# Optimization experiments

Measured on AMD Instinct MI355X. Metric: run time of the kernel, lower is better.

The kernel has to match this reference:

```python
import jax, jax.numpy as jnp
import numpy as np

B, T_IN, T_OUT, F, H = 1024, 168, 24, 8, 256


def _lstm_step(x, h, c, Wih, Whh, bih, bhh):
    # x: [B, in], h/c: [B, H]; PyTorch gate order i, f, g, o
    g = x @ Wih.T + h @ Whh.T + bih + bhh
    i, f, gg, o = jnp.split(g, 4, axis=-1)
    i = jax.nn.sigmoid(i)
    f = jax.nn.sigmoid(f)
    gg = jnp.tanh(gg)
    o = jax.nn.sigmoid(o)
    c2 = f * c + i * gg
    h2 = o * jnp.tanh(c2)
    return h2, c2


def _run_lstm(xs, Wih, Whh, bih, bhh):
    # xs: [T, B, in] -> (ys [T,B,H], h_T, c_T)
    Bs = xs.shape[1]
    h0 = jnp.zeros((Bs, H), xs.dtype)
    c0 = jnp.zeros((Bs, H), xs.dtype)
    def step(carry, x):
        h, c = carry
        h2, c2 = _lstm_step(x, h, c, Wih, Whh, bih, bhh)
        return (h2, c2), h2
    (hT, cT), ys = jax.lax.scan(step, (h0, c0), xs)
    return ys, hT, cT


def _forward(x, enc_Wih0, enc_Whh0, enc_bih0, enc_bhh0,
             enc_Wih1, enc_Whh1, enc_bih1, enc_bhh1,
             dec_Wih, dec_Whh, dec_bih, dec_bhh,
             fc1_W, fc1_b, attn_in_W, attn_in_b,
             attn_out_W, attn_out_b, fc2_W, fc2_b):
    scale = 1.0 / jnp.sqrt(jnp.asarray(H, x.dtype))

    # ---- encoder: 2-layer LSTM ----
    xs = jnp.transpose(x, (1, 0, 2))  # [T, B, F]
    ys0, h0, c0 = _run_lstm(xs, enc_Wih0, enc_Whh0, enc_bih0, enc_bhh0)
    _, h1, c1 = _run_lstm(ys0, enc_Wih1, enc_Whh1, enc_bih1, enc_bhh1)
    h_mean = (h0 + h1) * 0.5  # mean over layers, [B, H]
    c_mean = (c0 + c1) * 0.5

    # per-decoder initial state (same mean state for every decoder at t=0)
    h_state = jnp.tile(h_mean[None], (F, 1, 1))  # [F, B, H]
    c_state = jnp.tile(c_mean[None], (F, 1, 1))
    dec_in = x[:, -1, :]  # [B, F]

    def dec_one(xi, h, c, Wih, Whh, bih, bhh, f1W, f1b, inW, inb, oW, ob, f2W, f2b):
        # xi: [B, 1], single-feature single-step LSTM decode
        h2, c2 = _lstm_step(xi, h, c, Wih, Whh, bih, bhh)  # [B, H]
        a = jax.nn.leaky_relu(h2 @ f1W.T + f1b, 0.01)  # q = k = v
        qkv = a @ inW.T + inb  # [B, 3H]
        q, k, v = jnp.split(qkv, 3, axis=-1)
        # NB: faithful to the original bug: MultiheadAttention sees the batch
        # dim as the sequence dim, so attention is over the B examples.
        attn = jax.nn.softmax((q @ k.T) * scale, axis=-1)  # [B, B]
        ao = (attn @ v) @ oW.T + ob  # [B, H]
        out = jax.nn.leaky_relu(ao @ f2W.T + f2b, 0.01)  # [B, 1]
        return out[:, 0], h2, c2

    dec_all = jax.vmap(dec_one)  # over the F decoders

    def outer(carry, _):
        h, c, din = carry
        xi = din.T[:, :, None]  # [F, B, 1]
        out, h2, c2 = dec_all(xi, h, c, dec_Wih, dec_Whh, dec_bih, dec_bhh,
                              fc1_W, fc1_b, attn_in_W, attn_in_b,
                              attn_out_W, attn_out_b, fc2_W, fc2_b)
        return (h2, c2, out.T), out  # out: [F, B]

    _, outs = jax.lax.scan(outer, (h_state, c_state, dec_in), None, length=T_OUT)
    return jnp.transpose(outs, (2, 0, 1))  # [B, T_OUT, F]


def setup_inputs() -> dict:
    key = jax.random.key(0)
    ks = jax.random.split(key, 22)
    p = lambda k, shape: jax.random.normal(k, shape, dtype=jnp.float32) * 0.05
    return {
        "x": jax.random.normal(ks[0], (B, T_IN, F), dtype=jnp.float32),
        "enc_Wih0": p(ks[1], (4 * H, F)),
        "enc_Whh0": p(ks[2], (4 * H, H)),
        "enc_bih0": p(ks[3], (4 * H,)),
        "enc_bhh0": p(ks[4], (4 * H,)),
        "enc_Wih1": p(ks[5], (4 * H, H)),
        "enc_Whh1": p(ks[6], (4 * H, H)),
        "enc_bih1": p(ks[7], (4 * H,)),
        "enc_bhh1": p(ks[8], (4 * H,)),
        "dec_Wih": p(ks[9], (F, 4 * H, 1)),
        "dec_Whh": p(ks[10], (F, 4 * H, H)),
        "dec_bih": p(ks[11], (F, 4 * H)),
        "dec_bhh": p(ks[12], (F, 4 * H)),
        "fc1_W": p(ks[13], (F, H, H)),
        "fc1_b": p(ks[14], (F, H)),
        "attn_in_W": p(ks[15], (F, 3 * H, H)),
        "attn_in_b": p(ks[16], (F, 3 * H)),
        "attn_out_W": p(ks[17], (F, H, H)),
        "attn_out_b": p(ks[18], (F, H)),
        "fc2_W": p(ks[19], (F, 1, H)),
        "fc2_b": p(ks[20], (F, 1)),
    }


def reference(x, enc_Wih0, enc_Whh0, enc_bih0, enc_bhh0,
              enc_Wih1, enc_Whh1, enc_bih1, enc_bhh1,
              dec_Wih, dec_Whh, dec_bih, dec_bhh,
              fc1_W, fc1_b, attn_in_W, attn_in_b,
              attn_out_W, attn_out_b, fc2_W, fc2_b):
    return _forward(x, enc_Wih0, enc_Whh0, enc_bih0, enc_bhh0,
                    enc_Wih1, enc_Whh1, enc_bih1, enc_bhh1,
                    dec_Wih, dec_Whh, dec_bih, dec_bhh,
                    fc1_W, fc1_b, attn_in_W, attn_in_b,
                    attn_out_W, attn_out_b, fc2_W, fc2_b)
```

## Files before the change

### kernel.cpp

```cpp
#include <hip/hip_runtime.h>
#include <math.h>

#define H 256
#define H4 1024
#define Bsz 1024
#define TIN 168
#define TOUT 24
#define Fh 8
#define XROW (TIN*Fh)
#define BH ((size_t)Bsz * H)

typedef __attribute__((ext_vector_type(8))) short bf16x8;
typedef __attribute__((ext_vector_type(4))) float f32x4;

__device__ __forceinline__ ushort f2bf(float f) {
    union { float f; unsigned u; } v; v.f = f;
    unsigned r = v.u + 0x7fff + ((v.u >> 16) & 1);
    return (ushort)(r >> 16);
}
__device__ __forceinline__ float bf2f(ushort u) {
    union { unsigned u; float f; } v; v.u = ((unsigned)u) << 16;
    return v.f;
}
__device__ __forceinline__ float sigmf(float x) {
    return __fdividef(1.0f, 1.0f + __expf(-x));
}
__device__ __forceinline__ float tanhf_(float x) {
    const float e = __expf(-2.0f * fabsf(x));
    const float t = __fdividef(1.0f - e, 1.0f + e);
    return copysignf(t, x);
}

__device__ __forceinline__ void load_coh4(const ushort* p0, const ushort* p1,
                                          const ushort* p2, const ushort* p3,
                                          f32x4& a, f32x4& b, f32x4& c, f32x4& d)
{
    asm volatile(
        "global_load_dwordx4 %0, %4, off sc0 sc1\n\t"
        "global_load_dwordx4 %1, %5, off sc0 sc1\n\t"
        "global_load_dwordx4 %2, %6, off sc0 sc1\n\t"
        "global_load_dwordx4 %3, %7, off sc0 sc1\n\t"
        "s_waitcnt vmcnt(0)"
        : "=&v"(a), "=&v"(b), "=&v"(c), "=&v"(d)
        : "v"(p0), "v"(p1), "v"(p2), "v"(p3)
        : "memory");
}
__device__ __forceinline__ void load_coh8(const ushort* p0, const ushort* p1,
                                          const ushort* p2, const ushort* p3,
                                          const ushort* p4, const ushort* p5,
                                          const ushort* p6, const ushort* p7,
                                          f32x4& a, f32x4& b, f32x4& c, f32x4& d,
                                          f32x4& e, f32x4& f, f32x4& g, f32x4& h)
{
    asm volatile(
        "global_load_dwordx4 %0, %8, off sc0 sc1\n\t"
        "global_load_dwordx4 %1, %9, off sc0 sc1\n\t"
        "global_load_dwordx4 %2, %10, off sc0 sc1\n\t"
        "global_load_dwordx4 %3, %11, off sc0 sc1\n\t"
        "global_load_dwordx4 %4, %12, off sc0 sc1\n\t"
        "global_load_dwordx4 %5, %13, off sc0 sc1\n\t"
        "global_load_dwordx4 %6, %14, off sc0 sc1\n\t"
        "global_load_dwordx4 %7, %15, off sc0 sc1\n\t"
        "s_waitcnt vmcnt(0)"
        : "=&v"(a), "=&v"(b), "=&v"(c), "=&v"(d),
          "=&v"(e), "=&v"(f), "=&v"(g), "=&v"(h)
        : "v"(p0), "v"(p1), "v"(p2), "v"(p3), "v"(p4), "v"(p5), "v"(p6), "v"(p7)
        : "memory");
}
__device__ __forceinline__ void store_coh8B(ushort* p, uint2 v) {
    asm volatile("global_store_dwordx2 %0, %1, off sc0 sc1"
                 :: "v"(p), "v"(v) : "memory");
}

__device__ __forceinline__ void gbar2(unsigned* cnt, unsigned target) {
    asm volatile("s_waitcnt vmcnt(0)" ::: "memory");
    __syncthreads();
    if (threadIdx.x == 0) {
        __hip_atomic_fetch_add(cnt, 1u, __ATOMIC_RELAXED, __HIP_MEMORY_SCOPE_AGENT);
        int spins = 0;
        while (__hip_atomic_fetch_add(cnt, 0u, __ATOMIC_RELAXED,
                                      __HIP_MEMORY_SCOPE_AGENT) < target) {
            __builtin_amdgcn_s_sleep(1);
            if (++spins > 20000) break;
        }
    }
    __syncthreads();
    asm volatile("" ::: "memory");
}

__global__ __launch_bounds__(256)
void cast_f32_bf16(const float* __restrict__ in, ushort* __restrict__ out, int n) {
    int i = blockIdx.x * 256 + threadIdx.x;
    const int stride = gridDim.x * 256;
    for (; i < n; i += stride) out[i] = f2bf(in[i]);
}

__global__ __launch_bounds__(256)
void cast_pad_wih0(const float* __restrict__ in, ushort* __restrict__ out) {
    const int idx = blockIdx.x * 256 + threadIdx.x;
    const int row = idx >> 5, c = idx & 31;
    out[idx] = (c < 8) ? f2bf(in[row * 8 + c]) : (ushort)0;
}

__global__ __launch_bounds__(256)
void precompute_kernel(const float* __restrict__ oW, const float* __restrict__ ob,
                       const float* __restrict__ f2W, const float* __restrict__ f2b,
                       const float* __restrict__ inW, const float* __restrict__ inb,
                       float* __restrict__ u, float* __restrict__ dconst,
                       float* __restrict__ ccv)
{
    __shared__ float wsh[256];
    const int f = blockIdx.x;
    const int tid = threadIdx.x;
    float s = 0.f;
    for (int i = 0; i < 256; ++i)
        s += f2W[f * 256 + i] * oW[(size_t)f * 65536 + (size_t)i * 256 + tid];
    wsh[tid] = s;
    __syncthreads();
    float su = 0.f;
    for (int n = 0; n < 256; ++n)
        su += wsh[n] * inW[(size_t)f * 768 * 256 + (size_t)(512 + n) * 256 + tid];
    u[f * 256 + tid] = su;
    if (tid == 0) {
        float dd = 0.f, cc = 0.f;
        for (int n = 0; n < 256; ++n) dd += wsh[n] * inb[f * 768 + 512 + n];
        for (int i = 0; i < 256; ++i) cc += ob[f * 256 + i] * f2W[f * 256 + i];
        dconst[f] = dd;
        ccv[f] = cc + f2b[f];
    }
}

__global__ __launch_bounds__(256, 1)
void enc_persist2(const float* __restrict__ x,
                  const ushort* __restrict__ Whh0, const ushort* __restrict__ Wih0p,
                  const ushort* __restrict__ Wih1, const ushort* __restrict__ Whh1,
                  const float* __restrict__ bih0, const float* __restrict__ bhh0,
                  const float* __restrict__ bih1, const float* __restrict__ bhh1,
                  ushort* __restrict__ h0A, ushort* __restrict__ h0B,
                  ushort* __restrict__ h1A, ushort* __restrict__ h1B,
                  ushort* __restrict__ dh, float* __restrict__ dcb,
                  float* __restrict__ din, unsigned* __restrict__ bar)
{
    __shared__ ushort SA[32][264];
    __shared__ ushort SB[32][264];
    __shared__ ushort SC[32][264];
    __shared__ float pre[4][32][36];
    __shared__ ushort xL[32][32];

    const int tid = threadIdx.x;
    const int l = tid & 63;
    const int g = tid >> 6;
    const int lr = l & 15, lq = l >> 4, lk = lq * 8;
    const int grp = blockIdx.x >> 3, wgi = blockIdx.x & 7;
    const int rowbase = grp * 32;
    const int ub = wgi * 32;
    unsigned* cnt = bar + grp * 32;

    for (int e = tid; e < 32 * 32; e += 256) (&xL[0][0])[e] = 0;

    const int crow = tid >> 3;
    const int cu = (tid & 7) * 4;
    float c0v[4] = {0,0,0,0}, c1v[4] = {0,0,0,0};
    float h0v[4] = {0,0,0,0}, h1v[4] = {0,0,0,0};

    float b0s[2], b1s[2];
#pragma unroll
    for (int n = 0; n < 2; ++n) {
        const int j = ub + n * 16 + lr;
        b0s[n] = bih0[g * H + j] + bhh0[g * H + j];
        b1s[n] = bih1[g * H + j] + bhh1[g * H + j];
    }

    unsigned bph = 0;
    __syncthreads();

    for (int t = 0; t < TIN; ++t) {
        const int p = t & 1;
        const ushort* h0r = p ? h0B : h0A;
        ushort*       h0w = p ? h0A : h0B;
        const ushort* h1r = p ? h1B : h1A;
        ushort*       h1w = p ? h1A : h1B;

        {
            const ushort* src = h0r + rowbase * 256;
            f32x4 v0, v1, v2, v3;
            load_coh4(src + tid * 8, src + (tid + 256) * 8,
                      src + (tid + 512) * 8, src + (tid + 768) * 8, v0, v1, v2, v3);
            const int c16 = (tid & 31) * 8;
            *(f32x4*)&SA[tid >> 5][c16] = v0;
            *(f32x4*)&SA[(tid + 256) >> 5][c16] = v1;
            *(f32x4*)&SA[(tid + 512) >> 5][c16] = v2;
            *(f32x4*)&SA[(tid + 768) >> 5][c16] = v3;
            xL[tid >> 3][tid & 7] =
                f2bf(x[(size_t)(rowbase + (tid >> 3)) * XROW + t * Fh + (tid & 7)]);
        }
        __syncthreads();

        {
            bf16x8 am[2][8], ax[2];
#pragma unroll
            for (int m = 0; m < 2; ++m) {
#pragma unroll
                for (int k = 0; k < 8; ++k)
                    am[m][k] = *(const bf16x8*)&SA[m * 16 + lr][k * 32 + lk];
                ax[m] = *(const bf16x8*)&xL[m * 16 + lr][lk];
            }
            f32x4 acc[2][2] = {};
#pragma unroll
            for (int n = 0; n < 2; ++n) {
                const ushort* wp = Whh0 + (size_t)(g * H + ub + n * 16 + lr) * H + lk;
#pragma unroll
                for (int k = 0; k < 8; ++k) {
                    const bf16x8 b8 = *(const bf16x8*)(wp + k * 32);
                    acc[0][n] = __builtin_amdgcn_mfma_f32_16x16x32_bf16(am[0][k], b8, acc[0][n], 0, 0, 0);
                    acc[1][n] = __builtin_amdgcn_mfma_f32_16x16x32_bf16(am[1][k], b8, acc[1][n], 0, 0, 0);
                }
                const bf16x8 bx = *(const bf16x8*)(Wih0p + (size_t)(g * H + ub + n * 16 + lr) * 32 + lk);
                acc[0][n] = __builtin_amdgcn_mfma_f32_16x16x32_bf16(ax[0], bx, acc[0][n], 0, 0, 0);
                acc[1][n] = __builtin_amdgcn_mfma_f32_16x16x32_bf16(ax[1], bx, acc[1][n], 0, 0, 0);
            }
#pragma unroll
            for (int m = 0; m < 2; ++m)
#pragma unroll
                for (int n = 0; n < 2; ++n)
#pragma unroll
                    for (int r = 0; r < 4; ++r)
                        pre[g][m * 16 + lq * 4 + r][n * 16 + lr] = acc[m][n][r] + b0s[n];
        }
        __syncthreads();

        {
            const f32x4 pi = *(const f32x4*)&pre[0][crow][cu];
            const f32x4 pf = *(const f32x4*)&pre[1][crow][cu];
            const f32x4 pg = *(const f32x4*)&pre[2][crow][cu];
            const f32x4 po = *(const f32x4*)&pre[3][crow][cu];
#pragma unroll
            for (int j = 0; j < 4; ++j) {
                const float ig = sigmf(pi[j]);
                const float fg = sigmf(pf[j]);
                const float gg = tanhf_(pg[j]);
                const float og = sigmf(po[j]);
                c0v[j] = fg * c0v[j] + ig * gg;
                h0v[j] = og * tanhf_(c0v[j]);
            }
            uint2 hp;
            hp.x = (unsigned)f2bf(h0v[0]) | ((unsigned)f2bf(h0v[1]) << 16);
            hp.y = (unsigned)f2bf(h0v[2]) | ((unsigned)f2bf(h0v[3]) << 16);
            store_coh8B(h0w + (size_t)(rowbase + crow) * 256 + ub + cu, hp);
        }
        gbar2(cnt, ++bph * 8u);

        {
            const ushort* s0 = h0w + rowbase * 256;
            const ushort* s1 = h1r + rowbase * 256;
            f32x4 a0, a1, a2, a3, b0, b1, b2, b3;
            load_coh8(s0 + tid * 8, s0 + (tid + 256) * 8, s0 + (tid + 512) * 8, s0 + (tid + 768) * 8,
                      s1 + tid * 8, s1 + (tid + 256) * 8, s1 + (tid + 512) * 8, s1 + (tid + 768) * 8,
                      a0, a1, a2, a3, b0, b1, b2, b3);
            const int c16 = (tid & 31) * 8;
            *(f32x4*)&SB[tid >> 5][c16] = a0;
            *(f32x4*)&SB[(tid + 256) >> 5][c16] = a1;
            *(f32x4*)&SB[(tid + 512) >> 5][c16] = a2;
            *(f32x4*)&SB[(tid + 768) >> 5][c16] = a3;
            *(f32x4*)&SC[tid >> 5][c16] = b0;
            *(f32x4*)&SC[(tid + 256) >> 5][c16] = b1;
            *(f32x4*)&SC[(tid + 512) >> 5][c16] = b2;
            *(f32x4*)&SC[(tid + 768) >> 5][c16] = b3;
        }
        __syncthreads();

        {
            bf16x8 an[2][8], ah[2][8];
#pragma unroll
            for (int m = 0; m < 2; ++m)
#pragma unroll
                for (int k = 0; k < 8; ++k) {
                    an[m][k] = *(const bf16x8*)&SB[m * 16 + lr][k * 32 + lk];
                    ah[m][k] = *(const bf16x8*)&SC[m * 16 + lr][k * 32 + lk];
                }
            f32x4 acc[2][2] = {};
#pragma unroll
            for (int n = 0; n < 2; ++n) {
                const ushort* w1 = Wih1 + (size_t)(g * H + ub + n * 16 + lr) * H + lk;
                const ushort* w2 = Whh1 + (size_t)(g * H + ub + n * 16 + lr) * H + lk;
#pragma unroll
                for (int k = 0; k < 8; ++k) {
                    const bf16x8 b1 = *(const bf16x8*)(w1 + k * 32);
                    acc[0][n] = __builtin_amdgcn_mfma_f32_16x16x32_bf16(an[0][k], b1, acc[0][n], 0, 0, 0);
                    acc[1][n] = __builtin_amdgcn_mfma_f32_16x16x32_bf16(an[1][k], b1, acc[1][n], 0, 0, 0);
                    const bf16x8 b2 = *(const bf16x8*)(w2 + k * 32);
                    acc[0][n] = __builtin_amdgcn_mfma_f32_16x16x32_bf16(ah[0][k], b2, acc[0][n], 0, 0, 0);
                    acc[1][n] = __builtin_amdgcn_mfma_f32_16x16x32_bf16(ah[1][k], b2, acc[1][n], 0, 0, 0);
                }
            }
#pragma unroll
            for (int m = 0; m < 2; ++m)
#pragma unroll
                for (int n = 0; n < 2; ++n)
#pragma unroll
                    for (int r = 0; r < 4; ++r)
                        pre[g][m * 16 + lq * 4 + r][n * 16 + lr] = acc[m][n][r] + b1s[n];
        }
        __syncthreads();

        {
            const f32x4 pi = *(const f32x4*)&pre[0][crow][cu];
            const f32x4 pf = *(const f32x4*)&pre[1][crow][cu];
            const f32x4 pg = *(const f32x4*)&pre[2][crow][cu];
            const f32x4 po = *(const f32x4*)&pre[3][crow][cu];
#pragma unroll
            for (int j = 0; j < 4; ++j) {
                const float ig = sigmf(pi[j]);
                const float fg = sigmf(pf[j]);
                const float gg = tanhf_(pg[j]);
                const float og = sigmf(po[j]);
                c1v[j] = fg * c1v[j] + ig * gg;
                h1v[j] = og * tanhf_(c1v[j]);
            }
            uint2 hp;
            hp.x = (unsigned)f2bf(h1v[0]) | ((unsigned)f2bf(h1v[1]) << 16);
            hp.y = (unsigned)f2bf(h1v[2]) | ((unsigned)f2bf(h1v[3]) << 16);
            store_coh8B(h1w + (size_t)(rowbase + crow) * 256 + ub + cu, hp);
        }
        gbar2(cnt, ++bph * 8u);
    }

    {
        uint2 hm2;
        float cm[4];
        float hm[4];
#pragma unroll
        for (int j = 0; j < 4; ++j) {
            hm[j] = 0.5f * (h0v[j] + h1v[j]);
            cm[j] = 0.5f * (c0v[j] + c1v[j]);
        }
        hm2.x = (unsigned)f2bf(hm[0]) | ((unsigned)f2bf(hm[1]) << 16);
        hm2.y = (unsigned)f2bf(hm[2]) | ((unsigned)f2bf(hm[3]) << 16);
        const size_t idx = (size_t)(rowbase + crow) * 256 + ub + cu;
#pragma unroll
        for (int f = 0; f < Fh; ++f) {
            *(uint2*)&dh[f * BH + idx] = hm2;
            float4 c4; c4.x = cm[0]; c4.y = cm[1]; c4.z = cm[2]; c4.w = cm[3];
            *(float4*)&dcb[f * BH + idx] = c4;
        }
        if (wgi == 0) {
            const int r = tid >> 3, fc = tid & 7;
            din[(rowbase + r) * Fh + fc] =
                x[(size_t)(rowbase + r) * XROW + (TIN - 1) * Fh + fc];
        }
    }
}

template<int DO_ATTN, int DO_DEC>
__global__ __launch_bounds__(256, 1)
void dec_step(const ushort* __restrict__ qprev, const ushort* __restrict__ kprev,
              const float* __restrict__ vwprev,
              ushort* __restrict__ qcur, ushort* __restrict__ kcur,
              float* __restrict__ vwcur,
              ushort* __restrict__ dhg, float* __restrict__ dcg,
              const ushort* __restrict__ Whh, const float* __restrict__ Wih,
              const float* __restrict__ bih, const float* __restrict__ bhh,
              const ushort* __restrict__ f1Wb, const float* __restrict__ f1b,
              const ushort* __restrict__ inWb, const float* __restrict__ inb,
              const float* __restrict__ u, const float* __restrict__ dconst,
              const float* __restrict__ ccv, const float* __restrict__ din0,
              float* __restrict__ out, int t)
{
    __shared__ ushort h2s[32][264];
    __shared__ ushort as[32][264];
    __shared__ float dinL[32];
    __shared__ float tri[4][2][16][3];
    const int bid = blockIdx.x;
    const int f = bid & 7, mb = bid >> 3;
    const int m0 = mb * 32;
    const int tid = threadIdx.x;
    const int l = tid & 63, w = tid >> 6;
    const int lr = l & 15, lq = l >> 4, lk = lq * 8;

    if (DO_ATTN) {
        bf16x8 qf[2][8];
#pragma unroll
        for (int m = 0; m < 2; ++m)
#pragma unroll
            for (int k = 0; k < 8; ++k)
                qf[m][k] = *(const bf16x8*)(qprev + ((size_t)f * Bsz + m0 + m * 16 + lr) * H + k * 32 + lk);
        float mM0 = -1e30f, lS0 = 0.f, oS0 = 0.f;
        float mM1 = -1e30f, lS1 = 0.f, oS1 = 0.f;
        const int kb0 = w * 256;
        for (int kf = 0; kf < 16; ++kf) {
            const int kb = kb0 + kf * 16;
            f32x4 acc0 = {}, acc1 = {};
#pragma unroll
            for (int k = 0; k < 8; ++k) {
                const bf16x8 k8 = *(const bf16x8*)(kprev + ((size_t)f * Bsz + kb + lr) * H + k * 32 + lk);
                acc0 = __builtin_amdgcn_mfma_f32_16x16x32_bf16(k8, qf[0][k], acc0, 0, 0, 0);
                acc1 = __builtin_amdgcn_mfma_f32_16x16x32_bf16(k8, qf[1][k], acc1, 0, 0, 0);
            }
            const float4 v4 = *(const float4*)(vwprev + f * Bsz + kb + lq * 4);
            {
                const float mx = fmaxf(fmaxf(acc0[0], acc0[1]), fmaxf(acc0[2], acc0[3]));
                const float mn = fmaxf(mM0, mx);
                const float sc = __expf(mM0 - mn);
                const float e0 = __expf(acc0[0] - mn), e1 = __expf(acc0[1] - mn);
                const float e2 = __expf(acc0[2] - mn), e3 = __expf(acc0[3] - mn);
                lS0 = lS0 * sc + (e0 + e1 + e2 + e3);
                oS0 = oS0 * sc + (e0 * v4.x + e1 * v4.y + e2 * v4.z + e3 * v4.w);
                mM0 = mn;
            }
            {
                const float mx = fmaxf(fmaxf(acc1[0], acc1[1]), fmaxf(acc1[2], acc1[3]));
                const float mn = fmaxf(mM1, mx);
                const float sc = __expf(mM1 - mn);
                const float e0 = __expf(acc1[0] - mn), e1 = __expf(acc1[1] - mn);
                const float e2 = __expf(acc1[2] - mn), e3 = __expf(acc1[3] - mn);
                lS1 = lS1 * sc + (e0 + e1 + e2 + e3);
                oS1 = oS1 * sc + (e0 * v4.x + e1 * v4.y + e2 * v4.z + e3 * v4.w);
                mM1 = mn;
            }
        }
#pragma unroll
        for (int d = 16; d < 64; d <<= 1) {
            {
                const float m2 = __shfl_xor(mM0, d), l2 = __shfl_xor(lS0, d), o2 = __shfl_xor(oS0, d);
                const float mn = fmaxf(mM0, m2);
                const float sa = __expf(mM0 - mn), sb = __expf(m2 - mn);
                lS0 = lS0 * sa + l2 * sb; oS0 = oS0 * sa + o2 * sb; mM0 = mn;
            }
            {
                const float m2 = __shfl_xor(mM1, d), l2 = __shfl_xor(lS1, d), o2 = __shfl_xor(oS1, d);
                const float mn = fmaxf(mM1, m2);
                const float sa = __expf(mM1 - mn), sb = __expf(m2 - mn);
                lS1 = lS1 * sa + l2 * sb; oS1 = oS1 * sa + o2 * sb; mM1 = mn;
            }
        }
        if (l < 16) {
            tri[w][0][l][0] = mM0; tri[w][0][l][1] = lS0; tri[w][0][l][2] = oS0;
            tri[w][1][l][0] = mM1; tri[w][1][l][1] = lS1; tri[w][1][l][2] = oS1;
        }
        __syncthreads();
        if (tid < 32) {
            const int m = tid >> 4, qr = tid & 15;
            float M = tri[0][m][qr][0], L = tri[0][m][qr][1], O = tri[0][m][qr][2];
#pragma unroll
            for (int ww = 1; ww < 4; ++ww) {
                const float m2 = tri[ww][m][qr][0], l2 = tri[ww][m][qr][1], o2 = tri[ww][m][qr][2];
                const float mn = fmaxf(M, m2);
                const float sa = __expf(M - mn), sb = __expf(m2 - mn);
                L = L * sa + l2 * sb; O = O * sa + o2 * sb; M = mn;
            }
            float val = __fdividef(O, L) + ccv[f];
            val = (val > 0.f) ? val : 0.01f * val;
            const int b = m0 + m * 16 + qr;
            out[(size_t)b * (TOUT * Fh) + (size_t)(t - 1) * Fh + f] = val;
            dinL[m * 16 + qr] = val;
        }
        __syncthreads();
    }

    if (DO_DEC) {
        float bsum[4][4], wxr[4][4];
#pragma unroll
        for (int jt = 0; jt < 4; ++jt)
#pragma unroll
            for (int g = 0; g < 4; ++g) {
                const int j = w * 64 + jt * 16 + lr;
                bsum[jt][g] = bih[f * H4 + g * H + j] + bhh[f * H4 + g * H + j];
                wxr[jt][g] = Wih[f * H4 + g * H + j];
            }
        bf16x8 af[2][8];
#pragma unroll
        for (int m = 0; m < 2; ++m)
#pragma unroll
            for (int k = 0; k < 8; ++k)
                af[m][k] = *(const bf16x8*)(dhg + ((size_t)f * Bsz + m0 + m * 16 + lr) * H + k * 32 + lk);
        __syncthreads();
        const ushort* Wb = Whh + (size_t)f * (H4 * H);
#pragma unroll 1
        for (int jt = 0; jt < 4; ++jt) {
            const int jb = w * 64 + jt * 16;
            f32x4 acc[2][4] = {};
#pragma unroll
            for (int k = 0; k < 8; ++k)
#pragma unroll
                for (int g = 0; g < 4; ++g) {
                    const bf16x8 bf = *(const bf16x8*)(Wb + (size_t)(g * H + jb + lr) * H + k * 32 + lk);
                    acc[0][g] = __builtin_amdgcn_mfma_f32_16x16x32_bf16(af[0][k], bf, acc[0][g], 0, 0, 0);
                    acc[1][g] = __builtin_amdgcn_mfma_f32_16x16x32_bf16(af[1][k], bf, acc[1][g], 0, 0, 0);
                }
#pragma unroll
            for (int m = 0; m < 2; ++m)
#pragma unroll
                for (int r = 0; r < 4; ++r) {
                    const int row = m * 16 + lq * 4 + r;
                    const float xi = DO_ATTN ? dinL[row] : din0[(m0 + row) * Fh + f];
                    const float ig = sigmf(acc[m][0][r] + bsum[jt][0] + xi * wxr[jt][0]);
                    const float fg = sigmf(acc[m][1][r] + bsum[jt][1] + xi * wxr[jt][1]);
                    const float gg = tanhf_(acc[m][2][r] + bsum[jt][2] + xi * wxr[jt][2]);
                    const float og = sigmf(acc[m][3][r] + bsum[jt][3] + xi * wxr[jt][3]);
                    const size_t off = ((size_t)f * Bsz + m0 + row) * H + jb + lr;
                    const float cn = fg * dcg[off] + ig * gg;
                    dcg[off] = cn;
                    const ushort hb = f2bf(og * tanhf_(cn));
                    dhg[off] = hb;
                    h2s[row][jb + lr] = hb;
                }
        }
        __syncthreads();
        bf16x8 a2[2][8];
#pragma unroll
        for (int m = 0; m < 2; ++m)
#pragma unroll
            for (int k = 0; k < 8; ++k)
                a2[m][k] = *(const bf16x8*)&h2s[m * 16 + lr][k * 32 + lk];
        const ushort* Wf = f1Wb + (size_t)f * H * H;
#pragma unroll 1
        for (int nt = 0; nt < 4; ++nt) {
            const int n0 = w * 64 + nt * 16;
            f32x4 acc0 = {}, acc1 = {};
#pragma unroll
            for (int k = 0; k < 8; ++k) {
                const bf16x8 b8 = *(const bf16x8*)(Wf + (size_t)(n0 + lr) * H + k * 32 + lk);
                acc0 = __builtin_amdgcn_mfma_f32_16x16x32_bf16(a2[0][k], b8, acc0, 0, 0, 0);
                acc1 = __builtin_amdgcn_mfma_f32_16x16x32_bf16(a2[1][k], b8, acc1, 0, 0, 0);
            }
            const float bv = f1b[f * H + n0 + lr];
#pragma unroll
            for (int r = 0; r < 4; ++r) {
                float v0 = acc0[r] + bv; v0 = (v0 > 0.f) ? v0 : 0.01f * v0;
                as[lq * 4 + r][n0 + lr] = f2bf(v0);
                float v1 = acc1[r] + bv; v1 = (v1 > 0.f) ? v1 : 0.01f * v1;
                as[16 + lq * 4 + r][n0 + lr] = f2bf(v1);
            }
        }
        __syncthreads();
        bf16x8 a3[2][8];
#pragma unroll
        for (int m = 0; m < 2; ++m)
#pragma unroll
            for (int k = 0; k < 8; ++k)
                a3[m][k] = *(const bf16x8*)&as[m * 16 + lr][k * 32 + lk];
        const ushort* Wi = inWb + (size_t)f * 768 * H;
#pragma unroll 1
        for (int nt = 0; nt < 8; ++nt) {
            const int n0 = w * 128 + nt * 16;
            f32x4 acc0 = {}, acc1 = {};
#pragma unroll
            for (int k = 0; k < 8; ++k) {
                const bf16x8 b8 = *(const bf16x8*)(Wi + (size_t)(n0 + lr) * H + k * 32 + lk);
                acc0 = __builtin_amdgcn_mfma_f32_16x16x32_bf16(a3[0][k], b8, acc0, 0, 0, 0);
                acc1 = __builtin_amdgcn_mfma_f32_16x16x32_bf16(a3[1][k], b8, acc1, 0, 0, 0);
            }
            const float bv = inb[f * 768 + n0 + lr];
#pragma unroll
            for (int m = 0; m < 2; ++m)
#pragma unroll
                for (int r = 0; r < 4; ++r) {
                    const float v = (m ? acc1[r] : acc0[r]) + bv;
                    const int mrow = m0 + m * 16 + lq * 4 + r;
                    if (n0 < 256)
                        qcur[((size_t)f * Bsz + mrow) * H + n0 + lr] = f2bf(v * 0.0625f);
                    else
                        kcur[((size_t)f * Bsz + mrow) * H + n0 - 256 + lr] = f2bf(v);
                }
        }
        const float4 u4 = *(const float4*)(u + f * H + l * 4);
#pragma unroll 1
        for (int rr = 0; rr < 8; ++rr) {
            const int mloc = w * 8 + rr;
            const ushort4 a4 = *(const ushort4*)&as[mloc][l * 4];
            float s = bf2f(a4.x) * u4.x + bf2f(a4.y) * u4.y
                    + bf2f(a4.z) * u4.z + bf2f(a4.w) * u4.w;
#pragma unroll
            for (int d = 1; d < 64; d <<= 1) s += __shfl_xor(s, d);
            if (l == 0) vwcur[f * Bsz + m0 + mloc] = s + dconst[f];
        }
    }
}

extern "C" void kernel_launch(void* const* d_in, const int* in_sizes, int n_in,
                              void* d_out, int out_size, void* d_ws, size_t ws_size,
                              hipStream_t stream)
{
    const float* x     = (const float*)d_in[0];
    const float* eWih0 = (const float*)d_in[1];
    const float* eWhh0 = (const float*)d_in[2];
    const float* ebih0 = (const float*)d_in[3];
    const float* ebhh0 = (const float*)d_in[4];
    const float* eWih1 = (const float*)d_in[5];
    const float* eWhh1 = (const float*)d_in[6];
    const float* ebih1 = (const float*)d_in[7];
    const float* ebhh1 = (const float*)d_in[8];
    const float* dWih  = (const float*)d_in[9];
    const float* dWhh  = (const float*)d_in[10];
    const float* dbih  = (const float*)d_in[11];
    const float* dbhh  = (const float*)d_in[12];
    const float* f1W   = (const float*)d_in[13];
    const float* f1b   = (const float*)d_in[14];
    const float* inW   = (const float*)d_in[15];
    const float* inb   = (const float*)d_in[16];
    const float* oW    = (const float*)d_in[17];
    const float* ob    = (const float*)d_in[18];
    const float* f2W   = (const float*)d_in[19];
    const float* f2b   = (const float*)d_in[20];
    float* out = (float*)d_out;

    char* base = (char*)d_ws;
    size_t o = 0;
    auto alloc = [&](size_t bytes) { void* p = base + o; o += (bytes + 255) & ~(size_t)255; return p; };
    ushort* h0A = (ushort*)alloc(BH * 2);
    ushort* h1A = (ushort*)alloc(BH * 2);
    ushort* h0B = (ushort*)alloc(BH * 2);
    ushort* h1B = (ushort*)alloc(BH * 2);
    unsigned* bar = (unsigned*)alloc(32 * 32 * 4);
    ushort* qb[2]; ushort* kb[2]; float* vw[2];
    qb[0] = (ushort*)alloc(8 * BH * 2);
    qb[1] = (ushort*)alloc(8 * BH * 2);
    kb[0] = (ushort*)alloc(8 * BH * 2);
    kb[1] = (ushort*)alloc(8 * BH * 2);
    vw[0] = (float*)alloc((size_t)Fh * Bsz * 4);
    vw[1] = (float*)alloc((size_t)Fh * Bsz * 4);
    ushort* dhg  = (ushort*)alloc(8 * BH * 2);
    float*  dcg  = (float*)alloc(8 * BH * 4);
    float*  din0 = (float*)alloc((size_t)Bsz * Fh * 4);
    float*  ubuf = (float*)alloc((size_t)Fh * H * 4);
    float*  dbuf = (float*)alloc(Fh * 4);
    float*  ccb  = (float*)alloc(Fh * 4);
    ushort* wWhh0 = (ushort*)alloc((size_t)H4 * H * 2);
    ushort* wWih0p= (ushort*)alloc((size_t)H4 * 32 * 2);
    ushort* wWih1 = (ushort*)alloc((size_t)H4 * H * 2);
    ushort* wWhh1 = (ushort*)alloc((size_t)H4 * H * 2);
    ushort* wdWhh = (ushort*)alloc((size_t)8 * H4 * H * 2);
    ushort* wf1W  = (ushort*)alloc((size_t)8 * H * H * 2);
    ushort* winW  = (ushort*)alloc((size_t)8 * 768 * H * 2);

    const dim3 blk(256);

    hipMemsetAsync(d_ws, 0, BH * 2 * 2, stream);
    hipMemsetAsync(bar, 0, 32 * 32 * 4, stream);

    cast_f32_bf16<<<dim3(512), blk, 0, stream>>>(eWhh0, wWhh0, H4 * H);
    cast_f32_bf16<<<dim3(512), blk, 0, stream>>>(eWih1, wWih1, H4 * H);
    cast_f32_bf16<<<dim3(512), blk, 0, stream>>>(eWhh1, wWhh1, H4 * H);
    cast_pad_wih0<<<dim3(128), blk, 0, stream>>>(eWih0, wWih0p);
    cast_f32_bf16<<<dim3(1024), blk, 0, stream>>>(dWhh, wdWhh, 8 * H4 * H);
    cast_f32_bf16<<<dim3(512), blk, 0, stream>>>(f1W, wf1W, 8 * H * H);
    cast_f32_bf16<<<dim3(1024), blk, 0, stream>>>(inW, winW, 8 * 768 * H);
    precompute_kernel<<<dim3(8), blk, 0, stream>>>(oW, ob, f2W, f2b, inW, inb,
                                                   ubuf, dbuf, ccb);

    enc_persist2<<<dim3(256), blk, 0, stream>>>(
        x, wWhh0, wWih0p, wWih1, wWhh1, ebih0, ebhh0, ebih1, ebhh1,
        h0A, h0B, h1A, h1B, dhg, dcg, din0, bar);

    dec_step<0, 1><<<dim3(256), blk, 0, stream>>>(
        qb[1], kb[1], vw[1], qb[0], kb[0], vw[0], dhg, dcg,
        wdWhh, dWih, dbih, dbhh, wf1W, f1b, winW, inb,
        ubuf, dbuf, ccb, din0, out, 0);
    for (int t = 1; t < TOUT; ++t) {
        const int pp = (t - 1) & 1, pc = t & 1;
        dec_step<1, 1><<<dim3(256), blk, 0, stream>>>(
            qb[pp], kb[pp], vw[pp], qb[pc], kb[pc], vw[pc], dhg, dcg,
            wdWhh, dWih, dbih, dbhh, wf1W, f1b, winW, inb,
            ubuf, dbuf, ccb, din0, out, t);
    }
    dec_step<1, 0><<<dim3(256), blk, 0, stream>>>(
        qb[1], kb[1], vw[1], qb[0], kb[0], vw[0], dhg, dcg,
        wdWhh, dWih, dbih, dbhh, wf1W, f1b, winW, inb,
        ubuf, dbuf, ccb, din0, out, TOUT);

    (void)in_sizes; (void)n_in; (void)out_size; (void)ws_size;
}
```

Baseline: 3.681 ms.

## Merge encoder and decoder steps into one persistent kernel with grid barriers

Replaces the separate encoder kernel and the 25 per-step decoder launches with a single persistent kernel. Stages are separated by software global barriers instead of kernel boundaries. The hidden-state buffers move to a sliced layout so each thread loads one contiguous 32-element row. Decoder state is kept as one shared mean h/c buffer instead of eight replicated copies, and some loads now use L2-coherent rather than system-coherent flags. This removes per-launch overhead and the replicated state writes, but it depends on all 256 blocks being co-resident and on spin-barrier correctness.

Measured after the change: 3.568 ms. 1.03x faster.

```diff
diff --git a/kernel.cpp b/kernel.cpp
--- a/kernel.cpp
+++ b/kernel.cpp
@@ -9,6 +9,7 @@
 #define Fh 8
 #define XROW (TIN*Fh)
 #define BH ((size_t)Bsz * H)
+#define SL32 ((size_t)Bsz * 32)
 
 typedef __attribute__((ext_vector_type(8))) short bf16x8;
 typedef __attribute__((ext_vector_type(4))) float f32x4;
@@ -67,21 +68,68 @@
         : "v"(p0), "v"(p1), "v"(p2), "v"(p3), "v"(p4), "v"(p5), "v"(p6), "v"(p7)
         : "memory");
 }
+__device__ __forceinline__ void load_coh4f(const float* p0, const float* p1,
+                                           const float* p2, const float* p3,
+                                           float& a, float& b, float& c, float& d)
+{
+    asm volatile(
+        "global_load_dword %0, %4, off sc0 sc1\n\t"
+        "global_load_dword %1, %5, off sc0 sc1\n\t"
+        "global_load_dword %2, %6, off sc0 sc1\n\t"
+        "global_load_dword %3, %7, off sc0 sc1\n\t"
+        "s_waitcnt vmcnt(0)"
+        : "=&v"(a), "=&v"(b), "=&v"(c), "=&v"(d)
+        : "v"(p0), "v"(p1), "v"(p2), "v"(p3)
+        : "memory");
+}
 __device__ __forceinline__ void store_coh8B(ushort* p, uint2 v) {
     asm volatile("global_store_dwordx2 %0, %1, off sc0 sc1"
                  :: "v"(p), "v"(v) : "memory");
 }
-
-__device__ __forceinline__ void gbar2(unsigned* cnt, unsigned target) {
+__device__ __forceinline__ void store_coh16B(float* p, f32x4 v) {
+    asm volatile("global_store_dwordx4 %0, %1, off sc0 sc1"
+                 :: "v"(p), "v"(v) : "memory");
+}
+
+__device__ __forceinline__ void load_l2_8(const ushort* p0, const ushort* p1,
+                                          const ushort* p2, const ushort* p3,
+                                          const ushort* p4, const ushort* p5,
+                                          const ushort* p6, const ushort* p7,
+                                          f32x4& a, f32x4& b, f32x4& c, f32x4& d,
+                                          f32x4& e, f32x4& f, f32x4& g, f32x4& h)
+{
+    asm volatile(
+        "global_load_dwordx4 %0, %8, off sc0\n\t"
+        "global_load_dwordx4 %1, %9, off sc0\n\t"
+        "global_load_dwordx4 %2, %10, off sc0\n\t"
+        "global_load_dwordx4 %3, %11, off sc0\n\t"
+        "global_load_dwordx4 %4, %12, off sc0\n\t"
+        "global_load_dwordx4 %5, %13, off sc0\n\t"
+        "global_load_dwordx4 %6, %14, off sc0\n\t"
+        "global_load_dwordx4 %7, %15, off sc0\n\t"
+        "s_waitcnt vmcnt(0)"
+        : "=&v"(a), "=&v"(b), "=&v"(c), "=&v"(d),
+          "=&v"(e), "=&v"(f), "=&v"(g), "=&v"(h)
+        : "v"(p0), "v"(p1), "v"(p2), "v"(p3), "v"(p4), "v"(p5), "v"(p6), "v"(p7)
+        : "memory");
+}
+__device__ __forceinline__ void load_l2_f4(const float* p, f32x4& v) {
+    asm volatile(
+        "global_load_dwordx4 %0, %1, off sc0\n\t"
+        "s_waitcnt vmcnt(0)"
+        : "=&v"(v) : "v"(p) : "memory");
+}
+
+__device__ __forceinline__ void gbar(unsigned* cnt, unsigned target) {
     asm volatile("s_waitcnt vmcnt(0)" ::: "memory");
     __syncthreads();
     if (threadIdx.x == 0) {
         __hip_atomic_fetch_add(cnt, 1u, __ATOMIC_RELAXED, __HIP_MEMORY_SCOPE_AGENT);
-        int spins = 0;
+        int sp = 0;
         while (__hip_atomic_fetch_add(cnt, 0u, __ATOMIC_RELAXED,
                                       __HIP_MEMORY_SCOPE_AGENT) < target) {
-            __builtin_amdgcn_s_sleep(1);
-            if (++spins > 20000) break;
+            __builtin_amdgcn_s_sleep(2);
+            if (++sp > 20000) break;
         }
     }
     __syncthreads();
@@ -130,449 +178,484 @@
     }
 }
 
+struct MP {
+    const float *x, *ebih0, *ebhh0, *ebih1, *ebhh1;
+    const ushort *Whh0, *Wih0p, *Wih1, *Whh1;
+    ushort *h0A, *h0B, *h1A, *h1B, *hm;
+    float *cm;
+    const ushort *dWhh, *f1Wb, *inWb;
+    const float *dWih, *dbih, *dbhh, *f1b, *inb, *u, *dconst, *ccv;
+    ushort *kb0, *kb1;
+    float *vw0, *vw1, *out;
+    unsigned *bar;
+};
+
 __global__ __launch_bounds__(256, 1)
-void enc_persist2(const float* __restrict__ x,
-                  const ushort* __restrict__ Whh0, const ushort* __restrict__ Wih0p,
-                  const ushort* __restrict__ Wih1, const ushort* __restrict__ Whh1,
-                  const float* __restrict__ bih0, const float* __restrict__ bhh0,
-                  const float* __restrict__ bih1, const float* __restrict__ bhh1,
-                  ushort* __restrict__ h0A, ushort* __restrict__ h0B,
-                  ushort* __restrict__ h1A, ushort* __restrict__ h1B,
-                  ushort* __restrict__ dh, float* __restrict__ dcb,
-                  float* __restrict__ din, unsigned* __restrict__ bar)
+void mega2(MP P)
 {
     __shared__ ushort SA[32][264];
     __shared__ ushort SB[32][264];
     __shared__ ushort SC[32][264];
     __shared__ float pre[4][32][36];
     __shared__ ushort xL[32][32];
-
-    const int tid = threadIdx.x;
-    const int l = tid & 63;
-    const int g = tid >> 6;
-    const int lr = l & 15, lq = l >> 4, lk = lq * 8;
-    const int grp = blockIdx.x >> 3, wgi = blockIdx.x & 7;
-    const int rowbase = grp * 32;
-    const int ub = wgi * 32;
-    unsigned* cnt = bar + grp * 32;
-
-    for (int e = tid; e < 32 * 32; e += 256) (&xL[0][0])[e] = 0;
-
-    const int crow = tid >> 3;
-    const int cu = (tid & 7) * 4;
-    float c0v[4] = {0,0,0,0}, c1v[4] = {0,0,0,0};
-    float h0v[4] = {0,0,0,0}, h1v[4] = {0,0,0,0};
-
-    float b0s[2], b1s[2];
-#pragma unroll
-    for (int n = 0; n < 2; ++n) {
-        const int j = ub + n * 16 + lr;
-        b0s[n] = bih0[g * H + j] + bhh0[g * H + j];
-        b1s[n] = bih1[g * H + j] + bhh1[g * H + j];
-    }
-
-    unsigned bph = 0;
-    __syncthreads();
-
-    for (int t = 0; t < TIN; ++t) {
-        const int p = t & 1;
-        const ushort* h0r = p ? h0B : h0A;
-        ushort*       h0w = p ? h0A : h0B;
-        const ushort* h1r = p ? h1B : h1A;
-        ushort*       h1w = p ? h1A : h1B;
-
-        {
-            const ushort* src = h0r + rowbase * 256;
-            f32x4 v0, v1, v2, v3;
-            load_coh4(src + tid * 8, src + (tid + 256) * 8,
-                      src + (tid + 512) * 8, src + (tid + 768) * 8, v0, v1, v2, v3);
-            const int c16 = (tid & 31) * 8;
-            *(f32x4*)&SA[tid >> 5][c16] = v0;
-            *(f32x4*)&SA[(tid + 256) >> 5][c16] = v1;
-            *(f32x4*)&SA[(tid + 512) >> 5][c16] = v2;
-            *(f32x4*)&SA[(tid + 768) >> 5][c16] = v3;
-            xL[tid >> 3][tid & 7] =
-                f2bf(x[(size_t)(rowbase + (tid >> 3)) * XROW + t * Fh + (tid & 7)]);
-        }
-        __syncthreads();
-
-        {
-            bf16x8 am[2][8], ax[2];
-#pragma unroll
-            for (int m = 0; m < 2; ++m) {
-#pragma unroll
-                for (int k = 0; k < 8; ++k)
-                    am[m][k] = *(const bf16x8*)&SA[m * 16 + lr][k * 32 + lk];
-                ax[m] = *(const bf16x8*)&xL[m * 16 + lr][lk];
-            }
-            f32x4 acc[2][2] = {};
-#pragma unroll
-            for (int n = 0; n < 2; ++n) {
-                const ushort* wp = Whh0 + (size_t)(g * H + ub + n * 16 + lr) * H + lk;
-#pragma unroll
-                for (int k = 0; k < 8; ++k) {
-                    const bf16x8 b8 = *(const bf16x8*)(wp + k * 32);
-                    acc[0][n] = __builtin_amdgcn_mfma_f32_16x16x32_bf16(am[0][k], b8, acc[0][n], 0, 0, 0);
-                    acc[1][n] = __builtin_amdgcn_mfma_f32_16x16x32_bf16(am[1][k], b8, acc[1][n], 0, 0, 0);
-                }
-                const bf16x8 bx = *(const bf16x8*)(Wih0p + (size_t)(g * H + ub + n * 16 + lr) * 32 + lk);
-                acc[0][n] = __builtin_amdgcn_mfma_f32_16x16x32_bf16(ax[0], bx, acc[0][n], 0, 0, 0);
-                acc[1][n] = __builtin_amdgcn_mfma_f32_16x16x32_bf16(ax[1], bx, acc[1][n], 0, 0, 0);
-            }
-#pragma unroll
-            for (int m = 0; m < 2; ++m)
-#pragma unroll
-                for (int n = 0; n < 2; ++n)
-#pragma unroll
-                    for (int r = 0; r < 4; ++r)
-                        pre[g][m * 16 + lq * 4 + r][n * 16 + lr] = acc[m][n][r] + b0s[n];
-        }
-        __syncthreads();
-
-        {
-            const f32x4 pi = *(const f32x4*)&pre[0][crow][cu];
-            const f32x4 pf = *(const f32x4*)&pre[1][crow][cu];
-            const f32x4 pg = *(const f32x4*)&pre[2][crow][cu];
-            const f32x4 po = *(const f32x4*)&pre[3][crow][cu];
-#pragma unroll
-            for (int j = 0; j < 4; ++j) {
-                const float ig = sigmf(pi[j]);
-                const float fg = sigmf(pf[j]);
-                const float gg = tanhf_(pg[j]);
-                const float og = sigmf(po[j]);
-                c0v[j] = fg * c0v[j] + ig * gg;
-                h0v[j] = og * tanhf_(c0v[j]);
-            }
-            uint2 hp;
-            hp.x = (unsigned)f2bf(h0v[0]) | ((unsigned)f2bf(h0v[1]) << 16);
-            hp.y = (unsigned)f2bf(h0v[2]) | ((unsigned)f2bf(h0v[3]) << 16);
-            store_coh8B(h0w + (size_t)(rowbase + crow) * 256 + ub + cu, hp);
-        }
-        gbar2(cnt, ++bph * 8u);
-
-        {
-            const ushort* s0 = h0w + rowbase * 256;
-            const ushort* s1 = h1r + rowbase * 256;
-            f32x4 a0, a1, a2, a3, b0, b1, b2, b3;
-            load_coh8(s0 + tid * 8, s0 + (tid + 256) * 8, s0 + (tid + 512) * 8, s0 + (tid + 768) * 8,
-                      s1 + tid * 8, s1 + (tid + 256) * 8, s1 + (tid + 512) * 8, s1 + (tid + 768) * 8,
-                      a0, a1, a2, a3, b0, b1, b2, b3);
-            const int c16 = (tid & 31) * 8;
-            *(f32x4*)&SB[tid >> 5][c16] = a0;
-            *(f32x4*)&SB[(tid + 256) >> 5][c16] = a1;
-            *(f32x4*)&SB[(tid + 512) >> 5][c16] = a2;
-            *(f32x4*)&SB[(tid + 768) >> 5][c16] = a3;
-            *(f32x4*)&SC[tid >> 5][c16] = b0;
-            *(f32x4*)&SC[(tid + 256) >> 5][c16] = b1;
-            *(f32x4*)&SC[(tid + 512) >> 5][c16] = b2;
-            *(f32x4*)&SC[(tid + 768) >> 5][c16] = b3;
-        }
-        __syncthreads();
-
-        {
-            bf16x8 an[2][8], ah[2][8];
-#pragma unroll
-            for (int m = 0; m < 2; ++m)
-#pragma unroll
-                for (int k = 0; k < 8; ++k) {
-                    an[m][k] = *(const bf16x8*)&SB[m * 16 + lr][k * 32 + lk];
-                    ah[m][k] = *(const bf16x8*)&SC[m * 16 + lr][k * 32 + lk];
-                }
-            f32x4 acc[2][2] = {};
-#pragma unroll
-            for (int n = 0; n < 2; ++n) {
-                const ushort* w1 = Wih1 + (size_t)(g * H + ub + n * 16 + lr) * H + lk;
-                const ushort* w2 = Whh1 + (size_t)(g * H + ub + n * 16 + lr) * H + lk;
-#pragma unroll
-                for (int k = 0; k < 8; ++k) {
-                    const bf16x8 b1 = *(const bf16x8*)(w1 + k * 32);
-                    acc[0][n] = __builtin_amdgcn_mfma_f32_16x16x32_bf16(an[0][k], b1, acc[0][n], 0, 0, 0);
-                    acc[1][n] = __builtin_amdgcn_mfma_f32_16x16x32_bf16(an[1][k], b1, acc[1][n], 0, 0, 0);
-                    const bf16x8 b2 = *(const bf16x8*)(w2 + k * 32);
-                    acc[0][n] = __builtin_amdgcn_mfma_f32_16x16x32_bf16(ah[0][k], b2, acc[0][n], 0, 0, 0);
-                    acc[1][n] = __builtin_amdgcn_mfma_f32_16x16x32_bf16(ah[1][k], b2, acc[1][n], 0, 0, 0);
-                }
-            }
-#pragma unroll
-            for (int m = 0; m < 2; ++m)
-#pragma unroll
-                for (int n = 0; n < 2; ++n)
-#pragma unroll
-                    for (int r = 0; r < 4; ++r)
-                        pre[g][m * 16 + lq * 4 + r][n * 16 + lr] = acc[m][n][r] + b1s[n];
-        }
-        __syncthreads();
-
-        {
-            const f32x4 pi = *(const f32x4*)&pre[0][crow][cu];
-            const f32x4 pf = *(const f32x4*)&pre[1][crow][cu];
-            const f32x4 pg = *(const f32x4*)&pre[2][crow][cu];
-            const f32x4 po = *(const f32x4*)&pre[3][crow][cu];
-#pragma unroll
-            for (int j = 0; j < 4; ++j) {
-                const float ig = sigmf(pi[j]);
-                const float fg = sigmf(pf[j]);
-                const float gg = tanhf_(pg[j]);
-                const float og = sigmf(po[j]);
-                c1v[j] = fg * c1v[j] + ig * gg;
-                h1v[j] = og * tanhf_(c1v[j]);
-            }
-            uint2 hp;
-            hp.x = (unsigned)f2bf(h1v[0]) | ((unsigned)f2bf(h1v[1]) << 16);
-            hp.y = (unsigned)f2bf(h1v[2]) | ((unsigned)f2bf(h1v[3]) << 16);
-            store_coh8B(h1w + (size_t)(rowbase + crow) * 256 + ub + cu, hp);
-        }
-        gbar2(cnt, ++bph * 8u);
-    }
-
-    {
-        uint2 hm2;
-        float cm[4];
-        float hm[4];
-#pragma unroll
-        for (int j = 0; j < 4; ++j) {
-            hm[j] = 0.5f * (h0v[j] + h1v[j]);
-            cm[j] = 0.5f * (c0v[j] + c1v[j]);
-        }
-        hm2.x = (unsigned)f2bf(hm[0]) | ((unsigned)f2bf(hm[1]) << 16);
-        hm2.y = (unsigned)f2bf(hm[2]) | ((unsigned)f2bf(hm[3]) << 16);
-        const size_t idx = (size_t)(rowbase + crow) * 256 + ub + cu;
-#pragma unroll
-        for (int f = 0; f < Fh; ++f) {
-            *(uint2*)&dh[f * BH + idx] = hm2;
-            float4 c4; c4.x = cm[0]; c4.y = cm[1]; c4.z = cm[2]; c4.w = cm[3];
-            *(float4*)&dcb[f * BH + idx] = c4;
-        }
-        if (wgi == 0) {
-            const int r = tid >> 3, fc = tid & 7;
-            din[(rowbase + r) * Fh + fc] =
-                x[(size_t)(rowbase + r) * XROW + (TIN - 1) * Fh + fc];
-        }
-    }
-}
-
-template<int DO_ATTN, int DO_DEC>
-__global__ __launch_bounds__(256, 1)
-void dec_step(const ushort* __restrict__ qprev, const ushort* __restrict__ kprev,
-              const float* __restrict__ vwprev,
-              ushort* __restrict__ qcur, ushort* __restrict__ kcur,
-              float* __restrict__ vwcur,
-              ushort* __restrict__ dhg, float* __restrict__ dcg,
-              const ushort* __restrict__ Whh, const float* __restrict__ Wih,
-              const float* __restrict__ bih, const float* __restrict__ bhh,
-              const ushort* __restrict__ f1Wb, const float* __restrict__ f1b,
-              const ushort* __restrict__ inWb, const float* __restrict__ inb,
-              const float* __restrict__ u, const float* __restrict__ dconst,
-              const float* __restrict__ ccv, const float* __restrict__ din0,
-              float* __restrict__ out, int t)
-{
     __shared__ ushort h2s[32][264];
-    __shared__ ushort as[32][264];
+    __shared__ ushort as2[32][264];
+    __shared__ ushort qs[32][264];
+    __shared__ float tri[4][2][16][3];
     __shared__ float dinL[32];
-    __shared__ float tri[4][2][16][3];
+
     const int bid = blockIdx.x;
-    const int f = bid & 7, mb = bid >> 3;
-    const int m0 = mb * 32;
     const int tid = threadIdx.x;
     const int l = tid & 63, w = tid >> 6;
     const int lr = l & 15, lq = l >> 4, lk = lq * 8;
 
-    if (DO_ATTN) {
-        bf16x8 qf[2][8];
+    {
+        const int grp = bid >> 3, wgi = bid & 7;
+        const int rowbase = grp * 32;
+        const int ub = wgi * 32;
+        unsigned* cnt = P.bar + grp * 32;
+        const int g = w;
+        const int sS = tid >> 5, sR = tid & 31;
+
+        for (int e = tid; e < 32 * 32; e += 256) (&xL[0][0])[e] = 0;
+
+        const int crow = tid >> 3;
+        const int cu = (tid & 7) * 4;
+        float c0v[4] = {0,0,0,0}, c1v[4] = {0,0,0,0};
+        float h0v[4] = {0,0,0,0}, h1v[4] = {0,0,0,0};
+
+        float b0s[2], b1s[2];
+#pragma unroll
+        for (int n = 0; n < 2; ++n) {
+            const int j = ub + n * 16 + lr;
+            b0s[n] = P.ebih0[g * H + j] + P.ebhh0[g * H + j];
+            b1s[n] = P.ebih1[g * H + j] + P.ebhh1[g * H + j];
+        }
+        unsigned bph = 0;
+        __syncthreads();
+
+        for (int t = 0; t < TIN; ++t) {
+            const int p = t & 1;
+            const ushort* h0r = p ? P.h0B : P.h0A;
+            ushort*       h0w = p ? P.h0A : P.h0B;
+            const ushort* h1r = p ? P.h1B : P.h1A;
+            ushort*       h1w = p ? P.h1A : P.h1B;
+
+            {
+                const ushort* s0 = h0r + sS * SL32 + (size_t)(rowbase + sR) * 32;
+                f32x4 v0, v1, v2, v3;
+                load_coh4(s0, s0 + 8, s0 + 16, s0 + 24, v0, v1, v2, v3);
+                *(f32x4*)&SA[sR][sS * 32 + 0]  = v0;
+                *(f32x4*)&SA[sR][sS * 32 + 8]  = v1;
+                *(f32x4*)&SA[sR][sS * 32 + 16] = v2;
+                *(f32x4*)&SA[sR][sS * 32 + 24] = v3;
+                xL[tid >> 3][tid & 7] =
+                    f2bf(P.x[(size_t)(rowbase + (tid >> 3)) * XROW + t * Fh + (tid & 7)]);
+            }
+            __syncthreads();
+            {
+                bf16x8 am[2][8], ax[2];
+#pragma unroll
+                for (int m = 0; m < 2; ++m) {
+#pragma unroll
+                    for (int k = 0; k < 8; ++k)
+                        am[m][k] = *(const bf16x8*)&SA[m * 16 + lr][k * 32 + lk];
+                    ax[m] = *(const bf16x8*)&xL[m * 16 + lr][lk];
+                }
+                f32x4 acc[2][2] = {};
+#pragma unroll
+                for (int n = 0; n < 2; ++n) {
+                    const ushort* wp = P.Whh0 + (size_t)(g * H + ub + n * 16 + lr) * H + lk;
+#pragma unroll
+                    for (int k = 0; k < 8; ++k) {
+                        const bf16x8 b8 = *(const bf16x8*)(wp + k * 32);
+                        acc[0][n] = __builtin_amdgcn_mfma_f32_16x16x32_bf16(am[0][k], b8, acc[0][n], 0, 0, 0);
+                        acc[1][n] = __builtin_amdgcn_mfma_f32_16x16x32_bf16(am[1][k], b8, acc[1][n], 0, 0, 0);
+                    }
+                    const bf16x8 bx = *(const bf16x8*)(P.Wih0p + (size_t)(g * H + ub + n * 16 + lr) * 32 + lk);
+                    acc[0][n] = __builtin_amdgcn_mfma_f32_16x16x32_bf16(ax[0], bx, acc[0][n], 0, 0, 0);
+                    acc[1][n] = __builtin_amdgcn_mfma_f32_16x16x32_bf16(ax[1], bx, acc[1][n], 0, 0, 0);
+                }
+#pragma unroll
+                for (int m = 0; m < 2; ++m)
+#pragma unroll
+                    for (int n = 0; n < 2; ++n)
+#pragma unroll
+                        for (int r = 0; r < 4; ++r)
+                            pre[g][m * 16 + lq * 4 + r][n * 16 + lr] = acc[m][n][r] + b0s[n];
+            }
+            __syncthreads();
+            {
+                const f32x4 pi = *(const f32x4*)&pre[0][crow][cu];
+                const f32x4 pf = *(const f32x4*)&pre[1][crow][cu];
+                const f32x4 pg = *(const f32x4*)&pre[2][crow][cu];
+                const f32x4 po = *(const f32x4*)&pre[3][crow][cu];
+#pragma unroll
+                for (int j = 0; j < 4; ++j) {
+                    const float ig = sigmf(pi[j]);
+                    const float fg = sigmf(pf[j]);
+                    const float gg = tanhf_(pg[j]);
+                    const float og = sigmf(po[j]);
+                    c0v[j] = fg * c0v[j] + ig * gg;
+                    h0v[j] = og * tanhf_(c0v[j]);
+                }
+                uint2 hp;
+                hp.x = (unsigned)f2bf(h0v[0]) | ((unsigned)f2bf(h0v[1]) << 16);
+                hp.y = (unsigned)f2bf(h0v[2]) | ((unsigned)f2bf(h0v[3]) << 16);
+                store_coh8B(h0w + wgi * SL32 + (size_t)(rowbase + crow) * 32 + cu, hp);
+            }
+            gbar(cnt, ++bph * 8u);
+            {
+                const ushort* s0 = h0w + sS * SL32 + (size_t)(rowbase + sR) * 32;
+                const ushort* s1 = h1r + sS * SL32 + (size_t)(rowbase + sR) * 32;
+                f32x4 a0, a1, a2, a3, b0, b1, b2, b3;
+                load_coh8(s0, s0 + 8, s0 + 16, s0 + 24,
+                          s1, s1 + 8, s1 + 16, s1 + 24,
+                          a0, a1, a2, a3, b0, b1, b2, b3);
+                *(f32x4*)&SB[sR][sS * 32 + 0]  = a0;
+                *(f32x4*)&SB[sR][sS * 32 + 8]  = a1;
+                *(f32x4*)&SB[sR][sS * 32 + 16] = a2;
+                *(f32x4*)&SB[sR][sS * 32 + 24] = a3;
+                *(f32x4*)&SC[sR][sS * 32 + 0]  = b0;
+                *(f32x4*)&SC[sR][sS * 32 + 8]  = b1;
+                *(f32x4*)&SC[sR][sS * 32 + 16] = b2;
+                *(f32x4*)&SC[sR][sS * 32 + 24] = b3;
+            }
+            __syncthreads();
+            {
+                bf16x8 an[2][8], ah[2][8];
+#pragma unroll
+                for (int m = 0; m < 2; ++m)
+#pragma unroll
+                    for (int k = 0; k < 8; ++k) {
+                        an[m][k] = *(const bf16x8*)&SB[m * 16 + lr][k * 32 + lk];
+                        ah[m][k] = *(const bf16x8*)&SC[m * 16 + lr][k * 32 + lk];
+                    }
+                f32x4 acc[2][2] = {};
+#pragma unroll
+                for (int n = 0; n < 2; ++n) {
+                    const ushort* w1 = P.Wih1 + (size_t)(g * H + ub + n * 16 + lr) * H + lk;
+                    const ushort* w2 = P.Whh1 + (size_t)(g * H + ub + n * 16 + lr) * H + lk;
+#pragma unroll
+                    for (int k = 0; k < 8; ++k) {
+                        const bf16x8 b1 = *(const bf16x8*)(w1 + k * 32);
+                        acc[0][n] = __builtin_amdgcn_mfma_f32_16x16x32_bf16(an[0][k], b1, acc[0][n], 0, 0, 0);
+                        acc[1][n] = __builtin_amdgcn_mfma_f32_16x16x32_bf16(an[1][k], b1, acc[1][n], 0, 0, 0);
+                        const bf16x8 b2 = *(const bf16x8*)(w2 + k * 32);
+                        acc[0][n] = __builtin_amdgcn_mfma_f32_16x16x32_bf16(ah[0][k], b2, acc[0][n], 0, 0, 0);
+                        acc[1][n] = __builtin_amdgcn_mfma_f32_16x16x32_bf16(ah[1][k], b2, acc[1][n], 0, 0, 0);
+                    }
+                }
+#pragma unroll
+                for (int m = 0; m < 2; ++m)
+#pragma unroll
+                    for (int n = 0; n < 2; ++n)
+#pragma unroll
+                        for (int r = 0; r < 4; ++r)
+                            pre[g][m * 16 + lq * 4 + r][n * 16 + lr] = acc[m][n][r] + b1s[n];
+            }
+            __syncthreads();
+            {
+                const f32x4 pi = *(const f32x4*)&pre[0][crow][cu];
+                const f32x4 pf = *(const f32x4*)&pre[1][crow][cu];
+                const f32x4 pg = *(const f32x4*)&pre[2][crow][cu];
+                const f32x4 po = *(const f32x4*)&pre[3][crow][cu];
+#pragma unroll
+                for (int j = 0; j < 4; ++j) {
+                    const float ig = sigmf(pi[j]);
+                    const float fg = sigmf(pf[j]);
+                    const float gg = tanhf_(pg[j]);
+                    const float og = sigmf(po[j]);
+                    c1v[j] = fg * c1v[j] + ig * gg;
+                    h1v[j] = og * tanhf_(c1v[j]);
+                }
+                uint2 hp;
+                hp.x = (unsigned)f2bf(h1v[0]) | ((unsigned)f2bf(h1v[1]) << 16);
+                hp.y = (unsigned)f2bf(h1v[2]) | ((unsigned)f2bf(h1v[3]) << 16);
+                store_coh8B(h1w + wgi * SL32 + (size_t)(rowbase + crow) * 32 + cu, hp);
+            }
+            gbar(cnt, ++bph * 8u);
+        }
+        {
+            uint2 hp;
+            hp.x = (unsigned)f2bf(0.5f * (h0v[0] + h1v[0]))
+                 | ((unsigned)f2bf(0.5f * (h0v[1] + h1v[1])) << 16);
+            hp.y = (unsigned)f2bf(0.5f * (h0v[2] + h1v[2]))
+                 | ((unsigned)f2bf(0.5f * (h0v[3] + h1v[3])) << 16);
+            store_coh8B(P.hm + (size_t)(rowbase + crow) * 256 + ub + cu, hp);
+            f32x4 cv;
+#pragma unroll
+            for (int j = 0; j < 4; ++j) cv[j] = 0.5f * (c0v[j] + c1v[j]);
+            store_coh16B(P.cm + (size_t)(rowbase + crow) * 256 + ub + cu, cv);
+        }
+    }
+    gbar(P.bar + 2048, 256u);
+
+    {
+        const int f = bid & 7, mb = bid >> 3;
+        const int m0 = mb * 32;
+
+#pragma unroll
+        for (int it = 0; it < 4; ++it) {
+            const int idx = tid + it * 256;
+            const int r = idx >> 5, c16 = (idx & 31) * 8;
+            f32x4 v0, v1, v2, v3;
+            const ushort* pbase = P.hm + (size_t)(m0 + r) * 256 + c16;
+            asm volatile("global_load_dwordx4 %0, %1, off sc0 sc1\n\ts_waitcnt vmcnt(0)"
+                         : "=&v"(v0) : "v"(pbase) : "memory");
+            *(f32x4*)&h2s[r][c16] = v0;
+            (void)v1; (void)v2; (void)v3;
+        }
+        float cd[2][4][4];
 #pragma unroll
         for (int m = 0; m < 2; ++m)
 #pragma unroll
-            for (int k = 0; k < 8; ++k)
-                qf[m][k] = *(const bf16x8*)(qprev + ((size_t)f * Bsz + m0 + m * 16 + lr) * H + k * 32 + lk);
-        float mM0 = -1e30f, lS0 = 0.f, oS0 = 0.f;
-        float mM1 = -1e30f, lS1 = 0.f, oS1 = 0.f;
-        const int kb0 = w * 256;
-        for (int kf = 0; kf < 16; ++kf) {
-            const int kb = kb0 + kf * 16;
-            f32x4 acc0 = {}, acc1 = {};
-#pragma unroll
-            for (int k = 0; k < 8; ++k) {
-                const bf16x8 k8 = *(const bf16x8*)(kprev + ((size_t)f * Bsz + kb + lr) * H + k * 32 + lk);
-                acc0 = __builtin_amdgcn_mfma_f32_16x16x32_bf16(k8, qf[0][k], acc0, 0, 0, 0);
-                acc1 = __builtin_amdgcn_mfma_f32_16x16x32_bf16(k8, qf[1][k], acc1, 0, 0, 0);
-            }
-            const float4 v4 = *(const float4*)(vwprev + f * Bsz + kb + lq * 4);
-            {
-                const float mx = fmaxf(fmaxf(acc0[0], acc0[1]), fmaxf(acc0[2], acc0[3]));
-                const float mn = fmaxf(mM0, mx);
-                const float sc = __expf(mM0 - mn);
-                const float e0 = __expf(acc0[0] - mn), e1 = __expf(acc0[1] - mn);
-                const float e2 = __expf(acc0[2] - mn), e3 = __expf(acc0[3] - mn);
-                lS0 = lS0 * sc + (e0 + e1 + e2 + e3);
-                oS0 = oS0 * sc + (e0 * v4.x + e1 * v4.y + e2 * v4.z + e3 * v4.w);
-                mM0 = mn;
-            }
-            {
-                const float mx = fmaxf(fmaxf(acc1[0], acc1[1]), fmaxf(acc1[2], acc1[3]));
-                const float mn = fmaxf(mM1, mx);
-                const float sc = __expf(mM1 - mn);
-                const float e0 = __expf(acc1[0] - mn), e1 = __expf(acc1[1] - mn);
-                const float e2 = __expf(acc1[2] - mn), e3 = __expf(acc1[3] - mn);
-                lS1 = lS1 * sc + (e0 + e1 + e2 + e3);
-                oS1 = oS1 * sc + (e0 * v4.x + e1 * v4.y + e2 * v4.z + e3 * v4.w);
-                mM1 = mn;
-            }
-        }
-#pragma unroll
-        for (int d = 16; d < 64; d <<= 1) {
-            {
-                const float m2 = __shfl_xor(mM0, d), l2 = __shfl_xor(lS0, d), o2 = __shfl_xor(oS0, d);
-                const float mn = fmaxf(mM0, m2);
-                const float sa = __expf(mM0 - mn), sb = __expf(m2 - mn);
-                lS0 = lS0 * sa + l2 * sb; oS0 = oS0 * sa + o2 * sb; mM0 = mn;
-            }
-            {
-                const float m2 = __shfl_xor(mM1, d), l2 = __shfl_xor(lS1, d), o2 = __shfl_xor(oS1, d);
-                const float mn = fmaxf(mM1, m2);
-                const float sa = __expf(mM1 - mn), sb = __expf(m2 - mn);
-                lS1 = lS1 * sa + l2 * sb; oS1 = oS1 * sa + o2 * sb; mM1 = mn;
-            }
-        }
-        if (l < 16) {
-            tri[w][0][l][0] = mM0; tri[w][0][l][1] = lS0; tri[w][0][l][2] = oS0;
-            tri[w][1][l][0] = mM1; tri[w][1][l][1] = lS1; tri[w][1][l][2] = oS1;
-        }
-        __syncthreads();
-        if (tid < 32) {
-            const int m = tid >> 4, qr = tid & 15;
-            float M = tri[0][m][qr][0], L = tri[0][m][qr][1], O = tri[0][m][qr][2];
-#pragma unroll
-            for (int ww = 1; ww < 4; ++ww) {
-                const float m2 = tri[ww][m][qr][0], l2 = tri[ww][m][qr][1], o2 = tri[ww][m][qr][2];
-                const float mn = fmaxf(M, m2);
-                const float sa = __expf(M - mn), sb = __expf(m2 - mn);
-                L = L * sa + l2 * sb; O = O * sa + o2 * sb; M = mn;
-            }
-            float val = __fdividef(O, L) + ccv[f];
-            val = (val > 0.f) ? val : 0.01f * val;
-            const int b = m0 + m * 16 + qr;
-            out[(size_t)b * (TOUT * Fh) + (size_t)(t - 1) * Fh + f] = val;
-            dinL[m * 16 + qr] = val;
-        }
-        __syncthreads();
-    }
-
-    if (DO_DEC) {
+            for (int jt = 0; jt < 4; ++jt) {
+                const float* pc = P.cm + (size_t)(m0 + m * 16 + lq * 4) * 256
+                                + (w * 64 + jt * 16 + lr);
+                load_coh4f(pc, pc + 256, pc + 512, pc + 768,
+                           cd[m][jt][0], cd[m][jt][1], cd[m][jt][2], cd[m][jt][3]);
+            }
         float bsum[4][4], wxr[4][4];
 #pragma unroll
         for (int jt = 0; jt < 4; ++jt)
 #pragma unroll
             for (int g = 0; g < 4; ++g) {
                 const int j = w * 64 + jt * 16 + lr;
-                bsum[jt][g] = bih[f * H4 + g * H + j] + bhh[f * H4 + g * H + j];
-                wxr[jt][g] = Wih[f * H4 + g * H + j];
-            }
-        bf16x8 af[2][8];
-#pragma unroll
-        for (int m = 0; m < 2; ++m)
-#pragma unroll
-            for (int k = 0; k < 8; ++k)
-                af[m][k] = *(const bf16x8*)(dhg + ((size_t)f * Bsz + m0 + m * 16 + lr) * H + k * 32 + lk);
+                bsum[jt][g] = P.dbih[f * H4 + g * H + j] + P.dbhh[f * H4 + g * H + j];
+                wxr[jt][g] = P.dWih[f * H4 + g * H + j];
+            }
         __syncthreads();
-        const ushort* Wb = Whh + (size_t)f * (H4 * H);
-#pragma unroll 1
-        for (int jt = 0; jt < 4; ++jt) {
-            const int jb = w * 64 + jt * 16;
-            f32x4 acc[2][4] = {};
-#pragma unroll
-            for (int k = 0; k < 8; ++k)
-#pragma unroll
-                for (int g = 0; g < 4; ++g) {
-                    const bf16x8 bf = *(const bf16x8*)(Wb + (size_t)(g * H + jb + lr) * H + k * 32 + lk);
-                    acc[0][g] = __builtin_amdgcn_mfma_f32_16x16x32_bf16(af[0][k], bf, acc[0][g], 0, 0, 0);
-                    acc[1][g] = __builtin_amdgcn_mfma_f32_16x16x32_bf16(af[1][k], bf, acc[1][g], 0, 0, 0);
-                }
+
+        unsigned* fcnt = P.bar + 1024 + f * 32;
+
+        for (int t = 0; t < TOUT; ++t) {
+            ushort* kcur = (t & 1) ? P.kb1 : P.kb0;
+            float* vwcur = (t & 1) ? P.vw1 : P.vw0;
+
+            float xiv[2][4];
 #pragma unroll
             for (int m = 0; m < 2; ++m)
 #pragma unroll
                 for (int r = 0; r < 4; ++r) {
                     const int row = m * 16 + lq * 4 + r;
-                    const float xi = DO_ATTN ? dinL[row] : din0[(m0 + row) * Fh + f];
-                    const float ig = sigmf(acc[m][0][r] + bsum[jt][0] + xi * wxr[jt][0]);
-                    const float fg = sigmf(acc[m][1][r] + bsum[jt][1] + xi * wxr[jt][1]);
-                    const float gg = tanhf_(acc[m][2][r] + bsum[jt][2] + xi * wxr[jt][2]);
-                    const float og = sigmf(acc[m][3][r] + bsum[jt][3] + xi * wxr[jt][3]);
-                    const size_t off = ((size_t)f * Bsz + m0 + row) * H + jb + lr;
-                    const float cn = fg * dcg[off] + ig * gg;
-                    dcg[off] = cn;
-                    const ushort hb = f2bf(og * tanhf_(cn));
-                    dhg[off] = hb;
-                    h2s[row][jb + lr] = hb;
-                }
-        }
-        __syncthreads();
-        bf16x8 a2[2][8];
-#pragma unroll
-        for (int m = 0; m < 2; ++m)
-#pragma unroll
-            for (int k = 0; k < 8; ++k)
-                a2[m][k] = *(const bf16x8*)&h2s[m * 16 + lr][k * 32 + lk];
-        const ushort* Wf = f1Wb + (size_t)f * H * H;
+                    xiv[m][r] = (t == 0)
+                        ? P.x[(size_t)(m0 + row) * XROW + (TIN - 1) * Fh + f]
+                        : dinL[row];
+                }
+            bf16x8 af[2][8];
+#pragma unroll
+            for (int m = 0; m < 2; ++m)
+#pragma unroll
+                for (int k = 0; k < 8; ++k)
+                    af[m][k] = *(const bf16x8*)&h2s[m * 16 + lr][k * 32 + lk];
+            __syncthreads();
+            const ushort* Wb = P.dWhh + (size_t)f * (H4 * H);
 #pragma unroll 1
-        for (int nt = 0; nt < 4; ++nt) {
-            const int n0 = w * 64 + nt * 16;
-            f32x4 acc0 = {}, acc1 = {};
-#pragma unroll
-            for (int k = 0; k < 8; ++k) {
-                const bf16x8 b8 = *(const bf16x8*)(Wf + (size_t)(n0 + lr) * H + k * 32 + lk);
-                acc0 = __builtin_amdgcn_mfma_f32_16x16x32_bf16(a2[0][k], b8, acc0, 0, 0, 0);
-                acc1 = __builtin_amdgcn_mfma_f32_16x16x32_bf16(a2[1][k], b8, acc1, 0, 0, 0);
-            }
-            const float bv = f1b[f * H + n0 + lr];
-#pragma unroll
-            for (int r = 0; r < 4; ++r) {
-                float v0 = acc0[r] + bv; v0 = (v0 > 0.f) ? v0 : 0.01f * v0;
-                as[lq * 4 + r][n0 + lr] = f2bf(v0);
-                float v1 = acc1[r] + bv; v1 = (v1 > 0.f) ? v1 : 0.01f * v1;
-                as[16 + lq * 4 + r][n0 + lr] = f2bf(v1);
-            }
-        }
-        __syncthreads();
-        bf16x8 a3[2][8];
-#pragma unroll
-        for (int m = 0; m < 2; ++m)
-#pragma unroll
-            for (int k = 0; k < 8; ++k)
-                a3[m][k] = *(const bf16x8*)&as[m * 16 + lr][k * 32 + lk];
-        const ushort* Wi = inWb + (size_t)f * 768 * H;
+            for (int jt = 0; jt < 4; ++jt) {
+                const int j = w * 64 + jt * 16 + lr;
+                f32x4 acc[4][2] = {};
+#pragma unroll
+                for (int g = 0; g < 4; ++g) {
+                    const ushort* wp = Wb + (size_t)(g * H + j) * H + lk;
+#pragma unroll
+                    for (int k = 0; k < 8; ++k) {
+                        const bf16x8 b8 = *(const bf16x8*)(wp + k * 32);
+                        acc[g][0] = __builtin_amdgcn_mfma_f32_16x16x32_bf16(af[0][k], b8, acc[g][0], 0, 0, 0);
+                        acc[g][1] = __builtin_amdgcn_mfma_f32_16x16x32_bf16(af[1][k], b8, acc[g][1], 0, 0, 0);
+                    }
+                }
+#pragma unroll
+                for (int m = 0; m < 2; ++m)
+#pragma unroll
+                    for (int r = 0; r < 4; ++r) {
+                        const int row = m * 16 + lq * 4 + r;
+                        const float xi = xiv[m][r];
+                        const float ig = sigmf(acc[0][m][r] + bsum[jt][0] + xi * wxr[jt][0]);
+                        const float fg = sigmf(acc[1][m][r] + bsum[jt][1] + xi * wxr[jt][1]);
+                        const float gg = tanhf_(acc[2][m][r] + bsum[jt][2] + xi * wxr[jt][2]);
+                        const float og = sigmf(acc[3][m][r] + bsum[jt][3] + xi * wxr[jt][3]);
+                        const float cn = fg * cd[m][jt][r] + ig * gg;
+                        cd[m][jt][r] = cn;
+                        h2s[row][j] = f2bf(og * tanhf_(cn));
+                    }
+            }
+            __syncthreads();
+            bf16x8 a2[2][8];
+#pragma unroll
+            for (int m = 0; m < 2; ++m)
+#pragma unroll
+                for (int k = 0; k < 8; ++k)
+                    a2[m][k] = *(const bf16x8*)&h2s[m * 16 + lr][k * 32 + lk];
+            const ushort* Wf = P.f1Wb + (size_t)f * H * H;
 #pragma unroll 1
-        for (int nt = 0; nt < 8; ++nt) {
-            const int n0 = w * 128 + nt * 16;
-            f32x4 acc0 = {}, acc1 = {};
-#pragma unroll
-            for (int k = 0; k < 8; ++k) {
-                const bf16x8 b8 = *(const bf16x8*)(Wi + (size_t)(n0 + lr) * H + k * 32 + lk);
-                acc0 = __builtin_amdgcn_mfma_f32_16x16x32_bf16(a3[0][k], b8, acc0, 0, 0, 0);
-                acc1 = __builtin_amdgcn_mfma_f32_16x16x32_bf16(a3[1][k], b8, acc1, 0, 0, 0);
-            }
-            const float bv = inb[f * 768 + n0 + lr];
+            for (int nt = 0; nt < 4; ++nt) {
+                const int n = w * 64 + nt * 16 + lr;
+                f32x4 acc0 = {}, acc1 = {};
+                const ushort* wp = Wf + (size_t)n * H + lk;
+#pragma unroll
+                for (int k = 0; k < 8; ++k) {
+                    const bf16x8 b8 = *(const bf16x8*)(wp + k * 32);
+                    acc0 = __builtin_amdgcn_mfma_f32_16x16x32_bf16(a2[0][k], b8, acc0, 0, 0, 0);
+                    acc1 = __builtin_amdgcn_mfma_f32_16x16x32_bf16(a2[1][k], b8, acc1, 0, 0, 0);
+                }
+                const float bv = P.f1b[f * H + n];
+#pragma unroll
+                for (int r = 0; r < 4; ++r) {
+                    float v0 = acc0[r] + bv; v0 = (v0 > 0.f) ? v0 : 0.01f * v0;
+                    as2[lq * 4 + r][n] = f2bf(v0);
+                    float v1 = acc1[r] + bv; v1 = (v1 > 0.f) ? v1 : 0.01f * v1;
+                    as2[16 + lq * 4 + r][n] = f2bf(v1);
+                }
+            }
+            __syncthreads();
+            bf16x8 a3[2][8];
 #pragma unroll
             for (int m = 0; m < 2; ++m)
 #pragma unroll
-                for (int r = 0; r < 4; ++r) {
-                    const float v = (m ? acc1[r] : acc0[r]) + bv;
-                    const int mrow = m0 + m * 16 + lq * 4 + r;
-                    if (n0 < 256)
-                        qcur[((size_t)f * Bsz + mrow) * H + n0 + lr] = f2bf(v * 0.0625f);
-                    else
-                        kcur[((size_t)f * Bsz + mrow) * H + n0 - 256 + lr] = f2bf(v);
-                }
-        }
-        const float4 u4 = *(const float4*)(u + f * H + l * 4);
+                for (int k = 0; k < 8; ++k)
+                    a3[m][k] = *(const bf16x8*)&as2[m * 16 + lr][k * 32 + lk];
+            const ushort* Wi = P.inWb + (size_t)f * 768 * H;
 #pragma unroll 1
-        for (int rr = 0; rr < 8; ++rr) {
-            const int mloc = w * 8 + rr;
-            const ushort4 a4 = *(const ushort4*)&as[mloc][l * 4];
-            float s = bf2f(a4.x) * u4.x + bf2f(a4.y) * u4.y
-                    + bf2f(a4.z) * u4.z + bf2f(a4.w) * u4.w;
-#pragma unroll
-            for (int d = 1; d < 64; d <<= 1) s += __shfl_xor(s, d);
-            if (l == 0) vwcur[f * Bsz + m0 + mloc] = s + dconst[f];
+            for (int nt = 0; nt < 8; ++nt) {
+                const int n0 = w * 128 + nt * 16;
+                f32x4 acc0 = {}, acc1 = {};
+                const ushort* wp = Wi + (size_t)(n0 + lr) * H + lk;
+#pragma unroll
+                for (int k = 0; k < 8; ++k) {
+                    const bf16x8 b8 = *(const bf16x8*)(wp + k * 32);
+                    acc0 = __builtin_amdgcn_mfma_f32_16x16x32_bf16(a3[0][k], b8, acc0, 0, 0, 0);
+                    acc1 = __builtin_amdgcn_mfma_f32_16x16x32_bf16(a3[1][k], b8, acc1, 0, 0, 0);
+                }
+                const float bv = P.inb[f * 768 + n0 + lr];
+#pragma unroll
+                for (int m = 0; m < 2; ++m)
+#pragma unroll
+                    for (int r = 0; r < 4; ++r) {
+                        const float v = (m ? acc1[r] : acc0[r]) + bv;
+                        const int row = m * 16 + lq * 4 + r;
+                        if (n0 < 256)
+                            qs[row][n0 + lr] = f2bf(v * 0.0625f);
+                        else
+                            kcur[((size_t)f * Bsz + m0 + row) * H + n0 - 256 + lr] = f2bf(v);
+                    }
+            }
+            {
+                const float4 u4 = *(const float4*)(P.u + f * H + l * 4);
+#pragma unroll 1
+                for (int rr = 0; rr < 8; ++rr) {
+                    const int mloc = w * 8 + rr;
+                    const ushort4 a4 = *(const ushort4*)&as2[mloc][l * 4];
+                    float s = bf2f(a4.x) * u4.x + bf2f(a4.y) * u4.y
+                            + bf2f(a4.z) * u4.z + bf2f(a4.w) * u4.w;
+#pragma unroll
+                    for (int d = 1; d < 64; d <<= 1) s += __shfl_xor(s, d);
+                    if (l == 0) vwcur[f * Bsz + m0 + mloc] = s + P.dconst[f];
+                }
+            }
+            gbar(fcnt, (unsigned)(t + 1) * 32u);
+            {
+                bf16x8 qf[2][8];
+#pragma unroll
+                for (int m = 0; m < 2; ++m)
+#pragma unroll
+                    for (int k = 0; k < 8; ++k)
+                        qf[m][k] = *(const bf16x8*)&qs[m * 16 + lr][k * 32 + lk];
+                float mM0 = -1e30f, lS0 = 0.f, oS0 = 0.f;
+                float mM1 = -1e30f, lS1 = 0.f, oS1 = 0.f;
+                const int kb0r = w * 256;
+#pragma unroll 1
+                for (int kf = 0; kf < 16; ++kf) {
+                    const int kb = kb0r + kf * 16;
+                    const ushort* base = kcur + ((size_t)f * Bsz + kb + lr) * H + lk;
+                    f32x4 kr0, kr1, kr2, kr3, kr4, kr5, kr6, kr7;
+                    load_l2_8(base, base + 32, base + 64, base + 96,
+                              base + 128, base + 160, base + 192, base + 224,
+                              kr0, kr1, kr2, kr3, kr4, kr5, kr6, kr7);
+                    f32x4 acc0 = {}, acc1 = {};
+                    {
+                        const bf16x8 kk0 = *(bf16x8*)&kr0, kk1 = *(bf16x8*)&kr1,
+                                     kk2 = *(bf16x8*)&kr2, kk3 = *(bf16x8*)&kr3,
+                                     kk4 = *(bf16x8*)&kr4, kk5 = *(bf16x8*)&kr5,
+                                     kk6 = *(bf16x8*)&kr6, kk7 = *(bf16x8*)&kr7;
+                        acc0 = __builtin_amdgcn_mfma_f32_16x16x32_bf16(kk0, qf[0][0], acc0, 0, 0, 0);
+                        acc1 = __builtin_amdgcn_mfma_f32_16x16x32_bf16(kk0, qf[1][0], acc1, 0, 0, 0);
+                        acc0 = __builtin_amdgcn_mfma_f32_16x16x32_bf16(kk1, qf[0][1], acc0, 0, 0, 0);
+                        acc1 = __builtin_amdgcn_mfma_f32_16x16x32_bf16(kk1, qf[1][1], acc1, 0, 0, 0);
+                        acc0 = __builtin_amdgcn_mfma_f32_16x16x32_bf16(kk2, qf[0][2], acc0, 0, 0, 0);
+                        acc1 = __builtin_amdgcn_mfma_f32_16x16x32_bf16(kk2, qf[1][2], acc1, 0, 0, 0);
+                        acc0 = __builtin_amdgcn_mfma_f32_16x16x32_bf16(kk3, qf[0][3], acc0, 0, 0, 0);
+                        acc1 = __builtin_amdgcn_mfma_f32_16x16x32_bf16(kk3, qf[1][3], acc1, 0, 0, 0);
+                        acc0 = __builtin_amdgcn_mfma_f32_16x16x32_bf16(kk4, qf[0][4], acc0, 0, 0, 0);
+                        acc1 = __builtin_amdgcn_mfma_f32_16x16x32_bf16(kk4, qf[1][4], acc1, 0, 0, 0);
+                        acc0 = __builtin_amdgcn_mfma_f32_16x16x32_bf16(kk5, qf[0][5], acc0, 0, 0, 0);
+                        acc1 = __builtin_amdgcn_mfma_f32_16x16x32_bf16(kk5, qf[1][5], acc1, 0, 0, 0);
+                        acc0 = __builtin_amdgcn_mfma_f32_16x16x32_bf16(kk6, qf[0][6], acc0, 0, 0, 0);
+                        acc1 = __builtin_amdgcn_mfma_f32_16x16x32_bf16(kk6, qf[1][6], acc1, 0, 0, 0);
+                        acc0 = __builtin_amdgcn_mfma_f32_16x16x32_bf16(kk7, qf[0][7], acc0, 0, 0, 0);
+                        acc1 = __builtin_amdgcn_mfma_f32_16x16x32_bf16(kk7, qf[1][7], acc1, 0, 0, 0);
+                    }
+                    f32x4 v4w;
+                    load_l2_f4(vwcur + f * Bsz + kb + lq * 4, v4w);
+                    {
+                        const float mx = fmaxf(fmaxf(acc0[0], acc0[1]), fmaxf(acc0[2], acc0[3]));
+                        const float mn = fmaxf(mM0, mx);
+                        const float sc = __expf(mM0 - mn);
+                        const float e0 = __expf(acc0[0] - mn), e1 = __expf(acc0[1] - mn);
+                        const float e2 = __expf(acc0[2] - mn), e3 = __expf(acc0[3] - mn);
+                        lS0 = lS0 * sc + (e0 + e1 + e2 + e3);
+                        oS0 = oS0 * sc + (e0 * v4w[0] + e1 * v4w[1] + e2 * v4w[2] + e3 * v4w[3]);
+                        mM0 = mn;
+                    }
+                    {
+                        const float mx = fmaxf(fmaxf(acc1[0], acc1[1]), fmaxf(acc1[2], acc1[3]));
+                        const float mn = fmaxf(mM1, mx);
+                        const float sc = __expf(mM1 - mn);
+                        const float e0 = __expf(acc1[0] - mn), e1 = __expf(acc1[1] - mn);
+                        const float e2 = __expf(acc1[2] - mn), e3 = __expf(acc1[3] - mn);
+                        lS1 = lS1 * sc + (e0 + e1 + e2 + e3);
+                        oS1 = oS1 * sc + (e0 * v4w[0] + e1 * v4w[1] + e2 * v4w[2] + e3 * v4w[3]);
+                        mM1 = mn;
+                    }
+                }
+#pragma unroll
+                for (int d = 16; d < 64; d <<= 1) {
+                    {
+                        const float m2 = __shfl_xor(mM0, d), l2 = __shfl_xor(lS0, d), o2 = __shfl_xor(oS0, d);
+                        const float mn = fmaxf(mM0, m2);
+                        const float sa = __expf(mM0 - mn), sb = __expf(m2 - mn);
+                        lS0 = lS0 * sa + l2 * sb; oS0 = oS0 * sa + o2 * sb; mM0 = mn;
+                    }
+                    {
+                        const float m2 = __shfl_xor(mM1, d), l2 = __shfl_xor(lS1, d), o2 = __shfl_xor(oS1, d);
+                        const float mn = fmaxf(mM1, m2);
+                        const float sa = __expf(mM1 - mn), sb = __expf(m2 - mn);
+                        lS1 = lS1 * sa + l2 * sb; oS1 = oS1 * sa + o2 * sb; mM1 = mn;
+                    }
+                }
+                if (l < 16) {
+                    tri[w][0][l][0] = mM0; tri[w][0][l][1] = lS0; tri[w][0][l][2] = oS0;
+                    tri[w][1][l][0] = mM1; tri[w][1][l][1] = lS1; tri[w][1][l][2] = oS1;
+                }
+                __syncthreads();
+                if (tid < 32) {
+                    const int m = tid >> 4, qr = tid & 15;
+                    float M = tri[0][m][qr][0], L = tri[0][m][qr][1], O = tri[0][m][qr][2];
+#pragma unroll
+                    for (int ww = 1; ww < 4; ++ww) {
+                        const float m2 = tri[ww][m][qr][0], l2 = tri[ww][m][qr][1], o2 = tri[ww][m][qr][2];
+                        const float mn = fmaxf(M, m2);
+                        const float sa = __expf(M - mn), sb = __expf(m2 - mn);
+                        L = L * sa + l2 * sb; O = O * sa + o2 * sb; M = mn;
+                    }
+                    float val = __fdividef(O, L) + P.ccv[f];
+                    val = (val > 0.f) ? val : 0.01f * val;
+                    const int b = m0 + m * 16 + qr;
+                    P.out[(size_t)b * (TOUT * Fh) + (size_t)t * Fh + f] = val;
+                    dinL[m * 16 + qr] = val;
+                }
+                __syncthreads();
+            }
         }
     }
 }
@@ -602,7 +685,6 @@
     const float* ob    = (const float*)d_in[18];
     const float* f2W   = (const float*)d_in[19];
     const float* f2b   = (const float*)d_in[20];
-    float* out = (float*)d_out;
 
     char* base = (char*)d_ws;
     size_t o = 0;
@@ -611,20 +693,16 @@
     ushort* h1A = (ushort*)alloc(BH * 2);
     ushort* h0B = (ushort*)alloc(BH * 2);
     ushort* h1B = (ushort*)alloc(BH * 2);
-    unsigned* bar = (unsigned*)alloc(32 * 32 * 4);
-    ushort* qb[2]; ushort* kb[2]; float* vw[2];
-    qb[0] = (ushort*)alloc(8 * BH * 2);
-    qb[1] = (ushort*)alloc(8 * BH * 2);
-    kb[0] = (ushort*)alloc(8 * BH * 2);
-    kb[1] = (ushort*)alloc(8 * BH * 2);
-    vw[0] = (float*)alloc((size_t)Fh * Bsz * 4);
-    vw[1] = (float*)alloc((size_t)Fh * Bsz * 4);
-    ushort* dhg  = (ushort*)alloc(8 * BH * 2);
-    float*  dcg  = (float*)alloc(8 * BH * 4);
-    float*  din0 = (float*)alloc((size_t)Bsz * Fh * 4);
+    ushort* hm  = (ushort*)alloc(BH * 2);
+    float*  cm  = (float*)alloc(BH * 4);
+    ushort* kb0 = (ushort*)alloc(8 * BH * 2);
+    ushort* kb1 = (ushort*)alloc(8 * BH * 2);
+    float*  vw0 = (float*)alloc((size_t)Fh * Bsz * 4);
+    float*  vw1 = (float*)alloc((size_t)Fh * Bsz * 4);
     float*  ubuf = (float*)alloc((size_t)Fh * H * 4);
     float*  dbuf = (float*)alloc(Fh * 4);
     float*  ccb  = (float*)alloc(Fh * 4);
+    unsigned* bar = (unsigned*)alloc(3072 * 4);
     ushort* wWhh0 = (ushort*)alloc((size_t)H4 * H * 2);
     ushort* wWih0p= (ushort*)alloc((size_t)H4 * 32 * 2);
     ushort* wWih1 = (ushort*)alloc((size_t)H4 * H * 2);
@@ -636,7 +714,7 @@
     const dim3 blk(256);
 
     hipMemsetAsync(d_ws, 0, BH * 2 * 2, stream);
-    hipMemsetAsync(bar, 0, 32 * 32 * 4, stream);
+    hipMemsetAsync(bar, 0, 3072 * 4, stream);
 
     cast_f32_bf16<<<dim3(512), blk, 0, stream>>>(eWhh0, wWhh0, H4 * H);
     cast_f32_bf16<<<dim3(512), blk, 0, stream>>>(eWih1, wWih1, H4 * H);
@@ -648,25 +726,18 @@
     precompute_kernel<<<dim3(8), blk, 0, stream>>>(oW, ob, f2W, f2b, inW, inb,
                                                    ubuf, dbuf, ccb);
 
-    enc_persist2<<<dim3(256), blk, 0, stream>>>(
-        x, wWhh0, wWih0p, wWih1, wWhh1, ebih0, ebhh0, ebih1, ebhh1,
-        h0A, h0B, h1A, h1B, dhg, dcg, din0, bar);
-
-    dec_step<0, 1><<<dim3(256), blk, 0, stream>>>(
-        qb[1], kb[1], vw[1], qb[0], kb[0], vw[0], dhg, dcg,
-        wdWhh, dWih, dbih, dbhh, wf1W, f1b, winW, inb,
-        ubuf, dbuf, ccb, din0, out, 0);
-    for (int t = 1; t < TOUT; ++t) {
-        const int pp = (t - 1) & 1, pc = t & 1;
-        dec_step<1, 1><<<dim3(256), blk, 0, stream>>>(
-            qb[pp], kb[pp], vw[pp], qb[pc], kb[pc], vw[pc], dhg, dcg,
-            wdWhh, dWih, dbih, dbhh, wf1W, f1b, winW, inb,
-            ubuf, dbuf, ccb, din0, out, t);
-    }
-    dec_step<1, 0><<<dim3(256), blk, 0, stream>>>(
-        qb[1], kb[1], vw[1], qb[0], kb[0], vw[0], dhg, dcg,
-        wdWhh, dWih, dbih, dbhh, wf1W, f1b, winW, inb,
-        ubuf, dbuf, ccb, din0, out, TOUT);
+    MP P;
+    P.x = x; P.ebih0 = ebih0; P.ebhh0 = ebhh0; P.ebih1 = ebih1; P.ebhh1 = ebhh1;
+    P.Whh0 = wWhh0; P.Wih0p = wWih0p; P.Wih1 = wWih1; P.Whh1 = wWhh1;
+    P.h0A = h0A; P.h0B = h0B; P.h1A = h1A; P.h1B = h1B;
+    P.hm = hm; P.cm = cm;
+    P.dWhh = wdWhh; P.f1Wb = wf1W; P.inWb = winW;
+    P.dWih = dWih; P.dbih = dbih; P.dbhh = dbhh; P.f1b = f1b; P.inb = inb;
+    P.u = ubuf; P.dconst = dbuf; P.ccv = ccb;
+    P.kb0 = kb0; P.kb1 = kb1; P.vw0 = vw0; P.vw1 = vw1;
+    P.out = (float*)d_out; P.bar = bar;
+
+    mega2<<<dim3(256), blk, 0, stream>>>(P);
 
     (void)in_sizes; (void)n_in; (void)out_size; (void)ws_size;
 }
```
